# Kernel tuning notes

Measured on AMD Instinct MI355X. Metric: run time of the kernel, lower is better.

Reference implementation:

```python
import jax, jax.numpy as jnp
import numpy as np

B, N, C = 16, 1025, 768          # N = 32*32 patches + 1 CLS token
NUM_HEADS = 12
HEAD_DIM = C // NUM_HEADS        # 64
RED = 2                          # reduction_ratio
NEWTON_ITERS = 6


def setup_inputs() -> dict:
    key = jax.random.key(0)
    ks = jax.random.split(key, 5)
    return {
        "x": jax.random.normal(ks[0], (B, N, C), dtype=jnp.float32),
        "qkv_w": jax.random.normal(ks[1], (3 * C, C), dtype=jnp.float32) * 0.02,
        "qkv_b": jax.random.normal(ks[2], (3 * C,), dtype=jnp.float32) * 0.02,
        "proj_w": jax.random.normal(ks[3], (C, C), dtype=jnp.float32) * 0.02,
        "proj_b": jax.random.normal(ks[4], (C,), dtype=jnp.float32) * 0.02,
    }


def _kernel_gauss(x, y, tau):
    # exp(-||x-y||^2 / tau) via dot-product expansion; x:(B,H,N,D), y:(B,H,M,D)
    x_norm = jnp.sum(x * x, axis=-1, keepdims=True)          # (B,H,N,1)
    y_norm = jnp.sum(y * y, axis=-1, keepdims=True)          # (B,H,M,1)
    dot = jnp.einsum('bhnd,bhmd->bhnm', x, y)
    dist_sq = x_norm + jnp.swapaxes(y_norm, -2, -1) - 2.0 * dot
    return jnp.exp(-dist_sq / tau)


def _newton_inverse(mat, iters):
    # X_{k+1} = X_k (2I - A X_k); init X_0 = A^T / (||A||_inf^2 + eps)
    M = mat.shape[-1]
    I = jnp.eye(M, dtype=mat.dtype)
    norm = jnp.max(jnp.sum(jnp.abs(mat), axis=-1), axis=-1, keepdims=True)[..., None]  # (B,H,1,1)
    inv = jnp.swapaxes(mat, -2, -1) / (norm * norm + 1e-6)
    for _ in range(iters):
        inv = inv @ (2.0 * I - mat @ inv)
    return inv


def _spatial_pool(x, r):
    # avg-pool landmarks: (B,H,S*S,D) -> (B,H,(S//r)^2,D)
    b, h, n, d = x.shape
    s = int(round(n ** 0.5))
    sr = s // r
    x = x.reshape(b, h, sr, r, sr, r, d).mean(axis=(3, 5))
    return x.reshape(b, h, sr * sr, d)


def reference(x, qkv_w, qkv_b, proj_w, proj_b):
    b, n, c = x.shape
    tau = HEAD_DIM ** 0.5
    qkv = (x @ qkv_w.T + qkv_b).reshape(b, n, 3, NUM_HEADS, HEAD_DIM)
    qkv = jnp.transpose(qkv, (2, 0, 3, 1, 4))                # (3,B,H,N,D)
    q, k, v = qkv[0], qkv[1], qkv[2]
    q_cls, q_patch = q[:, :, :1], q[:, :, 1:]
    k_patch = k[:, :, 1:]
    v_patch = v[:, :, 1:]
    q_land = _spatial_pool(q_patch, RED)                     # (B,H,M,D)
    k_land = _spatial_pool(k_patch, RED)
    M1 = _kernel_gauss(q_patch, k_land, tau)                 # (B,H,N-1,M)
    M2 = _kernel_gauss(q_land, k_land, tau)                  # (B,H,M,M)
    M3 = _kernel_gauss(q_land, k_patch, tau)                 # (B,H,M,N-1)
    M2_inv = _newton_inverse(M2, NEWTON_ITERS)
    V_mixed = M2_inv @ (M3 @ v_patch)                        # (B,H,M,D)
    y_patch = M1 @ V_mixed                                   # (B,H,N-1,D)
    y_cls = _kernel_gauss(q_cls, k_land, tau) @ V_mixed      # (B,H,1,D)
    y = jnp.concatenate([y_cls, y_patch], axis=2)            # (B,H,N,D)
    y = jnp.swapaxes(y, 1, 2).reshape(b, n, c)
    return y @ proj_w.T + proj_b
```

## Files before the change

### kernel.cpp

```cpp
#include <hip/hip_runtime.h>

typedef unsigned short u16;

#define NBATCH 16
#define NHEADS 12
#define BH 192
#define NSEQ 1025
#define NP 1024
#define HD 64
#define LM 256
#define INV_TAU 0.125f
#define MROWS 16400
#define MT_X 1032
#define KB768 24
#define XS_ELE ((size_t)MT_X*KB768*64*8)

__device__ __forceinline__ float bf2f(u16 u){
  union { unsigned int i; float f; } x; x.i = ((unsigned int)u)<<16; return x.f;
}
__device__ __forceinline__ u16 f2bf(float f){
  union { float f; unsigned int i; } x; x.f = f;
  unsigned int r = x.i + 0x7fffu + ((x.i >> 16) & 1u);
  return (u16)(r >> 16);
}
__device__ __forceinline__ float ldf(const float* p){ return *p; }
__device__ __forceinline__ float ldf(const u16* p){ return bf2f(*p); }
__device__ __forceinline__ float4 ld4(const float* p){ return *(const float4*)p; }
__device__ __forceinline__ float4 ld4(const u16* p){
  uint2 u = *(const uint2*)p;
  return make_float4(bf2f((u16)u.x), bf2f((u16)(u.x>>16)),
                     bf2f((u16)u.y), bf2f((u16)(u.y>>16)));
}
__device__ __forceinline__ void stf(float* p, float v){ *p = v; }
__device__ __forceinline__ void stf(u16* p, float v){ *p = f2bf(v); }

typedef __attribute__((ext_vector_type(8))) short s8v;
typedef __attribute__((ext_vector_type(4))) float f4v;


__global__ __launch_bounds__(256) void probe_dtype(const u16* __restrict__ x, int* flag)
{
  __shared__ int cnt;
  if (threadIdx.x == 0) cnt = 0;
  __syncthreads();
  int c = 0;
  #pragma unroll
  for (int j = 0; j < 8; ++j){
    u16 u = x[2*(threadIdx.x*8 + j)];
    int e = (u >> 7) & 0xFF;
    if (e >= 100 && e <= 140) c++;
  }
  atomicAdd(&cnt, c);
  __syncthreads();
  if (threadIdx.x == 0) *flag = (cnt > 1024) ? 1 : 0;
}

template<typename TIN>
__global__ __launch_bounds__(256) void cvt_bias(
    const int* __restrict__ flag, int want,
    const TIN* __restrict__ bq_in, const TIN* __restrict__ bp_in,
    float* __restrict__ bq, float* __restrict__ bp)
{
  if (*flag != want) return;
  int i = blockIdx.x*256 + threadIdx.x;
  if (i < 2304) bq[i] = ldf(bq_in + i);
  if (i < 768)  bp[i] = ldf(bp_in + i);
}

template<typename TIN>
__global__ __launch_bounds__(256) void pack_ab(
    const int* __restrict__ flag, int want,
    const TIN* __restrict__ X, int rows_max, int tiles,
    u16* __restrict__ Dh, u16* __restrict__ Dl)
{
  if (*flag != want) return;
  int tid = blockIdx.x*256 + threadIdx.x;
  if (tid >= tiles*KB768*64) return;
  int lane = tid & 63;
  int kb = (tid >> 6) % KB768;
  int mt = tid / (KB768*64);
  int m = mt*16 + (lane & 15); if (m > rows_max-1) m = rows_max-1;
  int k = kb*32 + ((lane>>4) << 3);
  const TIN* src = X + (size_t)m*768 + k;
  float4 a = ld4(src), b = ld4(src + 4);
  float v[8] = {a.x,a.y,a.z,a.w,b.x,b.y,b.z,b.w};
  ushort4 h0,h1,l0,l1;
  u16 h;
  h=f2bf(v[0]); h0.x=h; l0.x=f2bf(v[0]-bf2f(h));
  h=f2bf(v[1]); h0.y=h; l0.y=f2bf(v[1]-bf2f(h));
  h=f2bf(v[2]); h0.z=h; l0.z=f2bf(v[2]-bf2f(h));
  h=f2bf(v[3]); h0.w=h; l0.w=f2bf(v[3]-bf2f(h));
  h=f2bf(v[4]); h1.x=h; l1.x=f2bf(v[4]-bf2f(h));
  h=f2bf(v[5]); h1.y=h; l1.y=f2bf(v[5]-bf2f(h));
  h=f2bf(v[6]); h1.z=h; l1.z=f2bf(v[6]-bf2f(h));
  h=f2bf(v[7]); h1.w=h; l1.w=f2bf(v[7]-bf2f(h));
  size_t o = (size_t)tid*8;
  *(ushort4*)(Dh+o)   = h0; *(ushort4*)(Dh+o+4) = h1;
  *(ushort4*)(Dl+o)   = l0; *(ushort4*)(Dl+o+4) = l1;
}

__global__ __launch_bounds__(256) void qkv_mfma(
    const u16* __restrict__ Xh, const u16* __restrict__ Xl,
    const u16* __restrict__ Wh, const u16* __restrict__ Wl,
    const float* __restrict__ bq,
    float* __restrict__ q, u16* __restrict__ kp, u16* __restrict__ vp)
{
  __shared__ u16 sAh[8*512], sAl[8*512], sBh[4*512], sBl[4*512];
  const int t = threadIdx.x, lane = t & 63, w = t >> 6;
  const int mt0 = blockIdx.x * 8;
  const int by  = blockIdx.y;
  const int nt0 = by * 4;
  const int wr = w >> 1, wc = w & 1;
  f4v acc[4][2];
  #pragma unroll
  for (int a=0;a<4;a++){ acc[a][0]=(f4v){0,0,0,0}; acc[a][1]=(f4v){0,0,0,0}; }
  for (int kb = 0; kb < KB768; ++kb){
    #pragma unroll
    for (int e = 0; e < 6; ++e){
      int cid = e*4 + w;
      const u16* src; u16* dst;
      if (cid < 16){
        int tile = cid >> 1;
        src = ((cid & 1) ? Xl : Xh) + ((size_t)(mt0 + tile)*KB768 + kb)*512 + lane*8;
        dst = ((cid & 1) ? sAl : sAh) + tile*512 + lane*8;
      } else {
        int bc = cid - 16; int tile = bc >> 1;
        src = ((bc & 1) ? Wl : Wh) + ((size_t)(nt0 + tile)*KB768 + kb)*512 + lane*8;
        dst = ((bc & 1) ? sBl : sBh) + tile*512 + lane*8;
      }
      *(uint4*)dst = *(const uint4*)src;
    }
    __syncthreads();
    s8v ah[4], al[4], bh2[2], bl2[2];
    #pragma unroll
    for (int i=0;i<4;i++){
      ah[i] = *(const s8v*)&sAh[(wr*4+i)*512 + lane*8];
      al[i] = *(const s8v*)&sAl[(wr*4+i)*512 + lane*8];
    }
    #pragma unroll
    for (int i=0;i<2;i++){
      bh2[i] = *(const s8v*)&sBh[(wc*2+i)*512 + lane*8];
      bl2[i] = *(const s8v*)&sBl[(wc*2+i)*512 + lane*8];
    }
    #pragma unroll
    for (int mi=0;mi<4;mi++)
      #pragma unroll
      for (int ni=0;ni<2;ni++){
        acc[mi][ni] = __builtin_amdgcn_mfma_f32_16x16x32_bf16(ah[mi], bh2[ni], acc[mi][ni],0,0,0);
        acc[mi][ni] = __builtin_amdgcn_mfma_f32_16x16x32_bf16(al[mi], bh2[ni], acc[mi][ni],0,0,0);
        acc[mi][ni] = __builtin_amdgcn_mfma_f32_16x16x32_bf16(ah[mi], bl2[ni], acc[mi][ni],0,0,0);
      }
    __syncthreads();
  }
  const int which = by / 12, h = by % 12;
  #pragma unroll
  for (int mi=0;mi<4;mi++)
    #pragma unroll
    for (int ni=0;ni<2;ni++){
      int d = (wc*2+ni)*16 + (lane & 15);
      float bias = bq[by*64 + d];
      int mbase = (mt0 + wr*4+mi)*16 + ((lane>>4)<<2);
      #pragma unroll
      for (int r=0;r<4;r++){
        int m = mbase + r;
        if (m >= MROWS) continue;
        float v = acc[mi][ni][r] + bias;
        int b = m / 1025, n = m - b*1025;
        if (which == 0) q[((size_t)(b*12+h)*1025 + n)*64 + d] = v;
        else if (n >= 1){
          size_t idx = ((size_t)(b*12+h)*1024 + (n-1))*64 + d;
          if (which == 1) kp[idx] = f2bf(v); else vp[idx] = f2bf(v);
        }
      }
    }
}

template<typename TOUT>
__global__ __launch_bounds__(256) void proj_mfma(
    const int* __restrict__ flag, int want,
    const u16* __restrict__ Yh, const u16* __restrict__ Yl,
    const u16* __restrict__ Wh, const u16* __restrict__ Wl,
    const float* __restrict__ bp, TOUT* __restrict__ Out)
{
  if (*flag != want) return;
  __shared__ u16 sAh[8*512], sAl[8*512], sBh[4*512], sBl[4*512];
  const int t = threadIdx.x, lane = t & 63, w = t >> 6;
  const int mt0 = blockIdx.x * 8;
  const int by  = blockIdx.y;
  const int nt0 = by * 4;
  const int wr = w >> 1, wc = w & 1;
  f4v acc[4][2];
  #pragma unroll
  for (int a=0;a<4;a++){ acc[a][0]=(f4v){0,0,0,0}; acc[a][1]=(f4v){0,0,0,0}; }
  for (int kb = 0; kb < KB768; ++kb){
    #pragma unroll
    for (int e = 0; e < 6; ++e){
      int cid = e*4 + w;
      const u16* src; u16* dst;
      if (cid < 16){
        int tile = cid >> 1;
        src = ((cid & 1) ? Yl : Yh) + ((size_t)(mt0 + tile)*KB768 + kb)*512 + lane*8;
        dst = ((cid & 1) ? sAl : sAh) + tile*512 + lane*8;
      } else {
        int bc = cid - 16; int tile = bc >> 1;
        src = ((bc & 1) ? Wl : Wh) + ((size_t)(nt0 + tile)*KB768 + kb)*512 + lane*8;
        dst = ((bc & 1) ? sBl : sBh) + tile*512 + lane*8;
      }
      *(uint4*)dst = *(const uint4*)src;
    }
    __syncthreads();
    s8v ah[4], al[4], bh2[2], bl2[2];
    #pragma unroll
    for (int i=0;i<4;i++){
      ah[i] = *(const s8v*)&sAh[(wr*4+i)*512 + lane*8];
      al[i] = *(const s8v*)&sAl[(wr*4+i)*512 + lane*8];
    }
    #pragma unroll
    for (int i=0;i<2;i++){
      bh2[i] = *(const s8v*)&sBh[(wc*2+i)*512 + lane*8];
      bl2[i] = *(const s8v*)&sBl[(wc*2+i)*512 + lane*8];
    }
    #pragma unroll
    for (int mi=0;mi<4;mi++)
      #pragma unroll
      for (int ni=0;ni<2;ni++){
        acc[mi][ni] = __builtin_amdgcn_mfma_f32_16x16x32_bf16(ah[mi], bh2[ni], acc[mi][ni],0,0,0);
        acc[mi][ni] = __builtin_amdgcn_mfma_f32_16x16x32_bf16(al[mi], bh2[ni], acc[mi][ni],0,0,0);
        acc[mi][ni] = __builtin_amdgcn_mfma_f32_16x16x32_bf16(ah[mi], bl2[ni], acc[mi][ni],0,0,0);
      }
    __syncthreads();
  }
  #pragma unroll
  for (int mi=0;mi<4;mi++)
    #pragma unroll
    for (int ni=0;ni<2;ni++){
      int d = (wc*2+ni)*16 + (lane & 15);
      int O = by*64 + d;
      float bias = bp[O];
      int mbase = (mt0 + wr*4+mi)*16 + ((lane>>4)<<2);
      #pragma unroll
      for (int r=0;r<4;r++){
        int m = mbase + r;
        if (m >= MROWS) continue;
        stf(Out + (size_t)m*768 + O, acc[mi][ni][r] + bias);
      }
    }
}

__global__ __launch_bounds__(256) void pack_newtA(
    const float* __restrict__ S, u16* __restrict__ Dh, u16* __restrict__ Dl)
{
  int tid = blockIdx.x*256 + threadIdx.x;
  int lane = tid & 63;
  int kb = (tid>>6) & 7;
  int mt = (tid>>9) & 15;
  int hd = tid >> 13;
  int m = mt*16 + (lane&15);
  int k = kb*32 + ((lane>>4)<<3);
  const float* src = S + (size_t)hd*65536 + m*256 + k;
  float4 a = *(const float4*)src, b = *(const float4*)(src+4);
  float v[8] = {a.x,a.y,a.z,a.w,b.x,b.y,b.z,b.w};
  ushort4 h0,h1,l0,l1; u16 h;
  h=f2bf(v[0]); h0.x=h; l0.x=f2bf(v[0]-bf2f(h));
  h=f2bf(v[1]); h0.y=h; l0.y=f2bf(v[1]-bf2f(h));
  h=f2bf(v[2]); h0.z=h; l0.z=f2bf(v[2]-bf2f(h));
  h=f2bf(v[3]); h0.w=h; l0.w=f2bf(v[3]-bf2f(h));
  h=f2bf(v[4]); h1.x=h; l1.x=f2bf(v[4]-bf2f(h));
  h=f2bf(v[5]); h1.y=h; l1.y=f2bf(v[5]-bf2f(h));
  h=f2bf(v[6]); h1.z=h; l1.z=f2bf(v[6]-bf2f(h));
  h=f2bf(v[7]); h1.w=h; l1.w=f2bf(v[7]-bf2f(h));
  size_t o = (size_t)hd*65536 + (size_t)((mt*8+kb)*64+lane)*8;
  *(ushort4*)(Dh+o)   = h0; *(ushort4*)(Dh+o+4) = h1;
  *(ushort4*)(Dl+o)   = l0; *(ushort4*)(Dl+o+4) = l1;
}

__global__ __launch_bounds__(256) void newton_initP(
    const float* __restrict__ M2g, const float* __restrict__ nrmg,
    u16* __restrict__ Ah, u16* __restrict__ Al,
    u16* __restrict__ Bh, u16* __restrict__ Bl)
{
  __shared__ float T[64][65];
  int hd = blockIdx.x, i0 = blockIdx.y*64, j0 = blockIdx.z*64;
  float nn = nrmg[hd];
  float sc = 1.0f/(nn*nn + 1e-6f);
  const float* Mb = M2g + (size_t)hd*65536;
  size_t hs = (size_t)hd*65536;
  int t = threadIdx.x;
  #pragma unroll
  for (int e=0;e<16;e++){ int f=e*256+t; int r=f>>6, c=f&63; T[r][c] = Mb[(i0+r)*256 + j0+c]; }
  __syncthreads();
  #pragma unroll
  for (int e=0;e<16;e++){
    int f=e*256+t; int r=f>>6, c=f&63;
    float v = T[c][r]*sc;
    int row = j0+r, col = i0+c;
    u16 hv = f2bf(v), lv = f2bf(v - bf2f(hv));
    size_t iA = hs + (size_t)(((row>>4)*8 + (col>>5))*64 + ((row&15)|(((col>>3)&3)<<4)))*8 + (col&7);
    Ah[iA]=hv; Al[iA]=lv;
    size_t iB = hs + (size_t)(((col>>4)*8 + (row>>5))*64 + ((col&15)|(((row>>3)&3)<<4)))*8 + (row&7);
    Bh[iB]=hv; Bl[iB]=lv;
  }
}

template<int MODE>
__global__ __launch_bounds__(256) void mgemmP(
    const u16* __restrict__ Ah_, const u16* __restrict__ Al_,
    const u16* __restrict__ Bh_, const u16* __restrict__ Bl_,
    u16* __restrict__ oAh, u16* __restrict__ oAl,
    u16* __restrict__ oBh, u16* __restrict__ oBl, float* __restrict__ oF)
{
  __shared__ u16 sAh[2048], sAl[2048], sBh[2048], sBl[2048];
  const int t = threadIdx.x, lane = t & 63, w = t >> 6;
  const int hd = blockIdx.x;
  const int mt0 = blockIdx.y * 4, nt0 = blockIdx.z * 4;
  const size_t hs = (size_t)hd * 65536;
  const int wr = w >> 1, wc = w & 1;
  f4v acc[2][2];
  acc[0][0]=(f4v){0,0,0,0}; acc[0][1]=(f4v){0,0,0,0};
  acc[1][0]=(f4v){0,0,0,0}; acc[1][1]=(f4v){0,0,0,0};
  for (int kb = 0; kb < 8; ++kb){
    #pragma unroll
    for (int e = 0; e < 4; ++e){
      int cid = e*4 + w;
      const u16* src; u16* dst;
      if (cid < 8){
        int tile = cid >> 1;
        src = ((cid & 1) ? Al_ : Ah_) + hs + (size_t)((mt0+tile)*8 + kb)*512 + lane*8;
        dst = ((cid & 1) ? sAl : sAh) + tile*512 + lane*8;
      } else {
        int bc = cid - 8; int tile = bc >> 1;
        src = ((bc & 1) ? Bl_ : Bh_) + hs + (size_t)((nt0+tile)*8 + kb)*512 + lane*8;
        dst = ((bc & 1) ? sBl : sBh) + tile*512 + lane*8;
      }
      *(uint4*)dst = *(const uint4*)src;
    }
    __syncthreads();
    s8v a_h[2], a_l[2], b_h[2], b_l[2];
    #pragma unroll
    for (int i=0;i<2;i++){
      a_h[i] = *(const s8v*)&sAh[(wr*2+i)*512 + lane*8];
      a_l[i] = *(const s8v*)&sAl[(wr*2+i)*512 + lane*8];
      b_h[i] = *(const s8v*)&sBh[(wc*2+i)*512 + lane*8];
      b_l[i] = *(const s8v*)&sBl[(wc*2+i)*512 + lane*8];
    }
    #pragma unroll
    for (int mi=0;mi<2;mi++)
      #pragma unroll
      for (int ni=0;ni<2;ni++){
        acc[mi][ni] = __builtin_amdgcn_mfma_f32_16x16x32_bf16(a_h[mi], b_h[ni], acc[mi][ni],0,0,0);
        acc[mi][ni] = __builtin_amdgcn_mfma_f32_16x16x32_bf16(a_l[mi], b_h[ni], acc[mi][ni],0,0,0);
        acc[mi][ni] = __builtin_amdgcn_mfma_f32_16x16x32_bf16(a_h[mi], b_l[ni], acc[mi][ni],0,0,0);
      }
    __syncthreads();
  }
  #pragma unroll
  for (int mi=0;mi<2;mi++)
    #pragma unroll
    for (int ni=0;ni<2;ni++){
      int col = (nt0 + wc*2+ni)*16 + (lane & 15);
      int rowb = (mt0 + wr*2+mi)*16 + ((lane>>4)<<2);
      #pragma unroll
      for (int r=0;r<4;r++){
        int row = rowb + r;
        float v = acc[mi][ni][r];
        if (MODE == 1) v = ((row==col)?2.0f:0.0f) - v;
        if (MODE == 2){
          oF[hs + (size_t)row*256 + col] = v;
        } else {
          u16 hv = f2bf(v), lv = f2bf(v - bf2f(hv));
          if (MODE == 0){
            size_t iA = hs + (size_t)(((row>>4)*8 + (col>>5))*64 + ((row&15)|(((col>>3)&3)<<4)))*8 + (col&7);
            oAh[iA]=hv; oAl[iA]=lv;
          }
          size_t iB = hs + (size_t)(((col>>4)*8 + (row>>5))*64 + ((col&15)|(((row>>3)&3)<<4)))*8 + (row&7);
          oBh[iB]=hv; oBl[iB]=lv;
        }
      }
    }
}

template<typename TIN>
__global__ __launch_bounds__(256) void xpool(
    const int* __restrict__ flag, int want,
    const TIN* __restrict__ X, float* __restrict__ XP)
{
  if (*flag != want) return;
  int idx = blockIdx.x*256 + threadIdx.x;
  if (idx >= NBATCH*LM*768) return;
  int c = idx % 768;
  int l = (idx / 768) & 255;
  int b = idx / (768*256);
  int lr = l >> 4, lc = l & 15;
  int p = lr*64 + lc*2;
  const TIN* xb = X + (size_t)b*NSEQ*768;
  XP[idx] = 0.25f*(ldf(xb + (size_t)(p+1)*768 + c) + ldf(xb + (size_t)(p+2)*768 + c)
                 + ldf(xb + (size_t)(p+33)*768 + c) + ldf(xb + (size_t)(p+34)*768 + c));
}

template<typename TIN>
__global__ __launch_bounds__(256) void lgemm(
    const int* __restrict__ flag, int want,
    const float* __restrict__ XP, const TIN* __restrict__ W, const TIN* __restrict__ Bias,
    int ob, float* __restrict__ OutL)
{
  if (*flag != want) return;
  __shared__ float As[16][68];
  __shared__ float Bs[16][68];
  const int t = threadIdx.x;
  const int m0 = blockIdx.x*64, o0 = blockIdx.y*64;
  const int tm = t>>4, tn = t&15;
  const int la_m = t>>2, la_k = (t&3)<<2;
  float acc[4][4] = {};
  const float* ap0 = XP + (size_t)(m0+la_m)*768 + la_k;
  const TIN* bp0 = W + (size_t)(ob+o0+la_m)*768 + la_k;
  for (int k0 = 0; k0 < 768; k0 += 16){
    float4 a4 = *(const float4*)(ap0 + k0);
    float4 b4 = ld4(bp0 + k0);
    As[la_k+0][la_m]=a4.x; As[la_k+1][la_m]=a4.y; As[la_k+2][la_m]=a4.z; As[la_k+3][la_m]=a4.w;
    Bs[la_k+0][la_m]=b4.x; Bs[la_k+1][la_m]=b4.y; Bs[la_k+2][la_m]=b4.z; Bs[la_k+3][la_m]=b4.w;
    __syncthreads();
    #pragma unroll
    for (int kk = 0; kk < 16; ++kk){
      float4 av = *(const float4*)&As[kk][tm<<2];
      float4 bv = *(const float4*)&Bs[kk][tn<<2];
      float ar[4]={av.x,av.y,av.z,av.w}, br[4]={bv.x,bv.y,bv.z,bv.w};
      #pragma unroll
      for (int ii=0;ii<4;ii++)
        #pragma unroll
        for (int jj=0;jj<4;jj++)
          acc[ii][jj] = fmaf(ar[ii], br[jj], acc[ii][jj]);
    }
    __syncthreads();
  }
  const int h = o0 >> 6;
  #pragma unroll
  for (int ii=0;ii<4;ii++){
    int m = m0 + (tm<<2) + ii;
    int b = m >> 8, l = m & 255;
    #pragma unroll
    for (int jj=0;jj<4;jj++){
      int d = (tn<<2) + jj;
      OutL[((size_t)(b*12+h)*256 + l)*64 + d] = acc[ii][jj] + ldf(Bias + ob + o0 + d);
    }
  }
}

template<typename TIN>
__global__ __launch_bounds__(256) void kvgemm(
    const int* __restrict__ flag, int want,
    const TIN* __restrict__ X, const TIN* __restrict__ W, const TIN* __restrict__ Bias,
    u16* __restrict__ kp, u16* __restrict__ vp)
{
  if (*flag != want) return;
  __shared__ float As[16][68];
  __shared__ float Bs[16][68];
  const int t = threadIdx.x;
  const int m0 = blockIdx.x*64, o0 = blockIdx.y*64;
  const int tm = t>>4, tn = t&15;
  const int la_m = t>>2, la_k = (t&3)<<2;
  float acc[4][4] = {};
  int ar = m0 + la_m;
  int arb = ar >> 10, arn = ar & 1023;
  const TIN* ap0 = X + (size_t)(arb*1025 + arn + 1)*768 + la_k;
  const TIN* bp0 = W + (size_t)(768 + o0 + la_m)*768 + la_k;
  for (int k0 = 0; k0 < 768; k0 += 16){
    float4 a4 = ld4(ap0 + k0);
    float4 b4 = ld4(bp0 + k0);
    As[la_k+0][la_m]=a4.x; As[la_k+1][la_m]=a4.y; As[la_k+2][la_m]=a4.z; As[la_k+3][la_m]=a4.w;
    Bs[la_k+0][la_m]=b4.x; Bs[la_k+1][la_m]=b4.y; Bs[la_k+2][la_m]=b4.z; Bs[la_k+3][la_m]=b4.w;
    __syncthreads();
    #pragma unroll
    for (int kk = 0; kk < 16; ++kk){
      float4 av = *(const float4*)&As[kk][tm<<2];
      float4 bv = *(const float4*)&Bs[kk][tn<<2];
      float arr[4]={av.x,av.y,av.z,av.w}, brr[4]={bv.x,bv.y,bv.z,bv.w};
      #pragma unroll
      for (int ii=0;ii<4;ii++)
        #pragma unroll
        for (int jj=0;jj<4;jj++)
          acc[ii][jj] = fmaf(arr[ii], brr[jj], acc[ii][jj]);
    }
    __syncthreads();
  }
  const int isv = (o0 >= 768);
  const int h = ((o0 - (isv ? 768 : 0)) >> 6);
  u16* dst = isv ? vp : kp;
  #pragma unroll
  for (int ii=0;ii<4;ii++){
    int m = m0 + (tm<<2) + ii;
    int b = m >> 10, n1 = m & 1023;
    #pragma unroll
    for (int jj=0;jj<4;jj++){
      int d = (tn<<2) + jj;
      dst[((size_t)(b*12+h)*1024 + n1)*64 + d] = f2bf(acc[ii][jj] + ldf(Bias + 768 + o0 + d));
    }
  }
}

template<typename TIN>
__global__ __launch_bounds__(256) void qgemm(
    const int* __restrict__ flag, int want,
    const TIN* __restrict__ X, const TIN* __restrict__ W, const TIN* __restrict__ Bias,
    float* __restrict__ q)
{
  if (*flag != want) return;
  __shared__ float As[16][68];
  __shared__ float Bs[16][68];
  const int t = threadIdx.x;
  const int m0 = blockIdx.x*64, o0 = blockIdx.y*64;
  const int tm = t>>4, tn = t&15;
  const int la_m = t>>2, la_k = (t&3)<<2;
  float acc[4][4] = {};
  int am = m0 + la_m; if (am > MROWS-1) am = MROWS-1;
  const TIN* ap0 = X + (size_t)am*768 + la_k;
  const TIN* bp0 = W + (size_t)(o0+la_m)*768 + la_k;
  for (int k0 = 0; k0 < 768; k0 += 16){
    float4 a4 = ld4(ap0 + k0);
    float4 b4 = ld4(bp0 + k0);
    As[la_k+0][la_m]=a4.x; As[la_k+1][la_m]=a4.y; As[la_k+2][la_m]=a4.z; As[la_k+3][la_m]=a4.w;
    Bs[la_k+0][la_m]=b4.x; Bs[la_k+1][la_m]=b4.y; Bs[la_k+2][la_m]=b4.z; Bs[la_k+3][la_m]=b4.w;
    __syncthreads();
    #pragma unroll
    for (int kk = 0; kk < 16; ++kk){
      float4 av = *(const float4*)&As[kk][tm<<2];
      float4 bv = *(const float4*)&Bs[kk][tn<<2];
      float arr[4]={av.x,av.y,av.z,av.w}, brr[4]={bv.x,bv.y,bv.z,bv.w};
      #pragma unroll
      for (int ii=0;ii<4;ii++)
        #pragma unroll
        for (int jj=0;jj<4;jj++)
          acc[ii][jj] = fmaf(arr[ii], brr[jj], acc[ii][jj]);
    }
    __syncthreads();
  }
  const int h = o0 >> 6;
  #pragma unroll
  for (int ii=0;ii<4;ii++){
    int m = m0 + (tm<<2) + ii;
    if (m >= MROWS) break;
    int b = m / 1025, n = m - b*1025;
    #pragma unroll
    for (int jj=0;jj<4;jj++){
      int d = (tn<<2) + jj;
      q[((size_t)(b*12+h)*1025 + n)*64 + d] = acc[ii][jj] + ldf(Bias + o0 + d);
    }
  }
}

template<typename TIN>
__global__ __launch_bounds__(256) void projgemm(
    const int* __restrict__ flag, int want,
    const float* __restrict__ Y, const TIN* __restrict__ W, const TIN* __restrict__ Bias,
    TIN* __restrict__ Out)
{
  if (*flag != want) return;
  __shared__ float As[16][68];
  __shared__ float Bs[16][68];
  const int t = threadIdx.x;
  const int m0 = blockIdx.x*64, o0 = blockIdx.y*64;
  const int tm = t>>4, tn = t&15;
  const int la_m = t>>2, la_k = (t&3)<<2;
  float acc[4][4] = {};
  int am = m0 + la_m; if (am > MROWS-1) am = MROWS-1;
  const float* ap0 = Y + (size_t)am*768 + la_k;
  const TIN* bp0 = W + (size_t)(o0+la_m)*768 + la_k;
  for (int k0 = 0; k0 < 768; k0 += 16){
    float4 a4 = *(const float4*)(ap0 + k0);
    float4 b4 = ld4(bp0 + k0);
    As[la_k+0][la_m]=a4.x; As[la_k+1][la_m]=a4.y; As[la_k+2][la_m]=a4.z; As[la_k+3][la_m]=a4.w;
    Bs[la_k+0][la_m]=b4.x; Bs[la_k+1][la_m]=b4.y; Bs[la_k+2][la_m]=b4.z; Bs[la_k+3][la_m]=b4.w;
    __syncthreads();
    #pragma unroll
    for (int kk = 0; kk < 16; ++kk){
      float4 av = *(const float4*)&As[kk][tm<<2];
      float4 bv = *(const float4*)&Bs[kk][tn<<2];
      float arr[4]={av.x,av.y,av.z,av.w}, brr[4]={bv.x,bv.y,bv.z,bv.w};
      #pragma unroll
      for (int ii=0;ii<4;ii++)
        #pragma unroll
        for (int jj=0;jj<4;jj++)
          acc[ii][jj] = fmaf(arr[ii], brr[jj], acc[ii][jj]);
    }
    __syncthreads();
  }
  #pragma unroll
  for (int ii=0;ii<4;ii++){
    int m = m0 + (tm<<2) + ii;
    if (m >= MROWS) break;
    #pragma unroll
    for (int jj=0;jj<4;jj++){
      int o = o0 + (tn<<2) + jj;
      stf(Out + (size_t)m*768 + o, acc[ii][jj] + ldf(Bias + o));
    }
  }
}

template<int MODE>
__global__ __launch_bounds__(256) void mgemm(
    const float* __restrict__ A, const float* __restrict__ B, float* __restrict__ C)
{
  __shared__ u16 Ah[4*64*8], Al[4*64*8];
  __shared__ u16 Bh[4*64*8], Bl[4*64*8];
  const int t = threadIdx.x;
  const int bh = blockIdx.x;
  const int i0 = blockIdx.y*64, j0 = blockIdx.z*64;
  const float* Ab = A + (size_t)bh*65536;
  const float* Bb = B + (size_t)bh*65536;
  float* Cb = C + (size_t)bh*65536;
  const int lane = t & 63, wave = t >> 6;
  const int wr = wave >> 1, wc = wave & 1;
  f4v acc[2][2];
  acc[0][0]=(f4v){0,0,0,0}; acc[0][1]=(f4v){0,0,0,0};
  acc[1][0]=(f4v){0,0,0,0}; acc[1][1]=(f4v){0,0,0,0};
  for (int k0 = 0; k0 < 256; k0 += 32){
    #pragma unroll
    for (int e = 0; e < 2; ++e){
      int f = e*256 + t;
      int r = f >> 3, c4 = (f & 7) << 2;
      float4 ga = *(const float4*)(Ab + (size_t)(i0+r)*256 + k0 + c4);
      int tile = r >> 4, m = r & 15, quad = c4 >> 3, jq = c4 & 7;
      int dst = ((tile*64 + quad*16 + m)*8 + jq);
      float va[4] = {ga.x, ga.y, ga.z, ga.w};
      ushort4 h4, l4; u16 h;
      h = f2bf(va[0]); h4.x = h; l4.x = f2bf(va[0]-bf2f(h));
      h = f2bf(va[1]); h4.y = h; l4.y = f2bf(va[1]-bf2f(h));
      h = f2bf(va[2]); h4.z = h; l4.z = f2bf(va[2]-bf2f(h));
      h = f2bf(va[3]); h4.w = h; l4.w = f2bf(va[3]-bf2f(h));
      *(ushort4*)&Ah[dst] = h4;
      *(ushort4*)&Al[dst] = l4;
    }
    #pragma unroll
    for (int e = 0; e < 2; ++e){
      int f = e*256 + t;
      int k = f >> 4, c4 = (f & 15) << 2;
      float4 gb = *(const float4*)(Bb + (size_t)(k0+k)*256 + j0 + c4);
      int quad = k >> 3, j = k & 7;
      float vb[4] = {gb.x, gb.y, gb.z, gb.w};
      #pragma unroll
      for (int s = 0; s < 4; ++s){
        int n = c4 + s;
        int idx = (((n>>4)*64 + quad*16 + (n&15))*8 + j);
        u16 h = f2bf(vb[s]);
        Bh[idx] = h;
        Bl[idx] = f2bf(vb[s] - bf2f(h));
      }
    }
    __syncthreads();
    s8v ah[2], al[2], bhf[2], blf[2];
    #pragma unroll
    for (int rt = 0; rt < 2; ++rt){
      int gt = wr*2 + rt;
      ah[rt] = *(const s8v*)&Ah[(gt*64 + lane)*8];
      al[rt] = *(const s8v*)&Al[(gt*64 + lane)*8];
    }
    #pragma unroll
    for (int ct = 0; ct < 2; ++ct){
      int gt = wc*2 + ct;
      bhf[ct] = *(const s8v*)&Bh[(gt*64 + lane)*8];
      blf[ct] = *(const s8v*)&Bl[(gt*64 + lane)*8];
    }
    #pragma unroll
    for (int rt = 0; rt < 2; ++rt)
      #pragma unroll
      for (int ct = 0; ct < 2; ++ct){
        acc[rt][ct] = __builtin_amdgcn_mfma_f32_16x16x32_bf16(ah[rt], bhf[ct], acc[rt][ct], 0,0,0);
        acc[rt][ct] = __builtin_amdgcn_mfma_f32_16x16x32_bf16(al[rt], bhf[ct], acc[rt][ct], 0,0,0);
        acc[rt][ct] = __builtin_amdgcn_mfma_f32_16x16x32_bf16(ah[rt], blf[ct], acc[rt][ct], 0,0,0);
      }
    __syncthreads();
  }
  #pragma unroll
  for (int rt = 0; rt < 2; ++rt)
    #pragma unroll
    for (int ct = 0; ct < 2; ++ct){
      int col = j0 + (wc*2+ct)*16 + (lane & 15);
      int rbase = i0 + (wr*2+rt)*16 + (lane >> 4)*4;
      #pragma unroll
      for (int r = 0; r < 4; ++r){
        int row = rbase + r;
        float v = acc[rt][ct][r];
        if (MODE == 1) v = ((row==col) ? 2.0f : 0.0f) - v;
        Cb[(size_t)row*256 + col] = v;
      }
    }
}

template<int MODE, int NDIM>
__global__ __launch_bounds__(256) void bgemm(
    const float* __restrict__ A, const float* __restrict__ B, float* __restrict__ C)
{
  __shared__ float As[16][68];
  __shared__ float Bs[16][68];
  const int t = threadIdx.x;
  const int bh = blockIdx.x;
  const int i0 = blockIdx.y*64, j0 = blockIdx.z*64;
  const int tm = t>>4, tn = t&15;
  const float* Ab = A + (size_t)bh*65536;
  const float* Bb = B + (size_t)bh*256*NDIM;
  float* Cb = C + (size_t)bh*256*NDIM;
  const int la_m = t>>2, la_k = (t&3)<<2;
  const int lb_k = t>>4, lb_n = (t&15)<<2;
  float acc[4][4] = {};
  for (int k0 = 0; k0 < 256; k0 += 16){
    float4 a4 = *(const float4*)(Ab + (i0+la_m)*256 + k0 + la_k);
    As[la_k+0][la_m]=a4.x; As[la_k+1][la_m]=a4.y; As[la_k+2][la_m]=a4.z; As[la_k+3][la_m]=a4.w;
    *(float4*)&Bs[lb_k][lb_n] = *(const float4*)(Bb + (k0+lb_k)*NDIM + j0 + lb_n);
    __syncthreads();
    #pragma unroll
    for (int kk = 0; kk < 16; ++kk){
      float4 av = *(const float4*)&As[kk][tm<<2];
      float4 bv = *(const float4*)&Bs[kk][tn<<2];
      float arr[4]={av.x,av.y,av.z,av.w}, brr[4]={bv.x,bv.y,bv.z,bv.w};
      #pragma unroll
      for (int ii=0;ii<4;ii++)
        #pragma unroll
        for (int jj=0;jj<4;jj++)
          acc[ii][jj] = fmaf(arr[ii], brr[jj], acc[ii][jj]);
    }
    __syncthreads();
  }
  #pragma unroll
  for (int ii=0;ii<4;ii++){
    int i = i0 + (tm<<2) + ii;
    #pragma unroll
    for (int jj=0;jj<4;jj++){
      int j = j0 + (tn<<2) + jj;
      float v = acc[ii][jj];
      if (MODE == 1) v = ((i==j) ? 2.0f : 0.0f) - v;
      Cb[i*NDIM + j] = v;
    }
  }
}

__global__ __launch_bounds__(256) void gauss_m2(
    const float* __restrict__ Q, const float* __restrict__ K,
    const float* __restrict__ qn, const float* __restrict__ kn, float* __restrict__ Out)
{
  __shared__ float Qs[64][68];
  __shared__ float Kst[64][66];
  const int bh = blockIdx.x, i0 = blockIdx.y*64, j0 = blockIdx.z*64;
  const int t = threadIdx.x, tm = t>>4, tn = t&15;
  #pragma unroll
  for (int e=0;e<4;e++){
    int f = e*256 + t; int r = f>>4; int c4 = (f&15)<<2;
    *(float4*)&Qs[r][c4] = *(const float4*)(Q + (size_t)(bh*256 + i0 + r)*64 + c4);
    float4 k4 = *(const float4*)(K + (size_t)(bh*256 + j0 + r)*64 + c4);
    Kst[c4+0][r]=k4.x; Kst[c4+1][r]=k4.y; Kst[c4+2][r]=k4.z; Kst[c4+3][r]=k4.w;
  }
  __syncthreads();
  float d[4][4] = {};
  for (int k0=0;k0<64;k0+=4){
    float qv[4][4], kv[4][4];
    #pragma unroll
    for (int ii=0;ii<4;ii++){
      float4 q4 = *(const float4*)&Qs[(tm<<2)+ii][k0];
      qv[ii][0]=q4.x; qv[ii][1]=q4.y; qv[ii][2]=q4.z; qv[ii][3]=q4.w;
    }
    #pragma unroll
    for (int kk=0;kk<4;kk++)
      #pragma unroll
      for (int jj=0;jj<4;jj++)
        kv[kk][jj] = Kst[k0+kk][(tn<<2)+jj];
    #pragma unroll
    for (int ii=0;ii<4;ii++)
      #pragma unroll
      for (int jj=0;jj<4;jj++){
        d[ii][jj] = fmaf(qv[ii][0], kv[0][jj], d[ii][jj]);
        d[ii][jj] = fmaf(qv[ii][1], kv[1][jj], d[ii][jj]);
        d[ii][jj] = fmaf(qv[ii][2], kv[2][jj], d[ii][jj]);
        d[ii][jj] = fmaf(qv[ii][3], kv[3][jj], d[ii][jj]);
      }
  }
  float qnr[4], knc[4];
  #pragma unroll
  for (int ii=0;ii<4;ii++) qnr[ii] = qn[bh*256 + i0 + (tm<<2) + ii];
  #pragma unroll
  for (int jj=0;jj<4;jj++) knc[jj] = kn[bh*256 + j0 + (tn<<2) + jj];
  #pragma unroll
  for (int ii=0;ii<4;ii++)
    #pragma unroll
    for (int jj=0;jj<4;jj++)
      Out[(size_t)(bh*256 + i0 + (tm<<2) + ii)*256 + j0 + (tn<<2) + jj] =
        __expf(-(qnr[ii] + knc[jj] - 2.0f*d[ii][jj]) * INV_TAU);
}

template<int YMODE, int RQ, int RK, typename TQ, typename TK, typename TV>
__global__ __launch_bounds__(256) void gauss_av(
    const TQ* __restrict__ Q, const TK* __restrict__ Km,
    const TV* __restrict__ V, const float* __restrict__ qn,
    const float* __restrict__ kn, float* __restrict__ Out)
{
  __shared__ float Qs[64][68];
  __shared__ float Kst[64][66];
  __shared__ float Ss[64][68];
  const int bh = blockIdx.x, i0 = blockIdx.y*64;
  const int t = threadIdx.x, tm = t>>4, tn = t&15;
  #pragma unroll
  for (int e=0;e<4;e++){
    int f = e*256 + t; int r = f>>4; int c4 = (f&15)<<2;
    int gi = i0 + r; if (gi > RQ-1) gi = RQ-1;
    *(float4*)&Qs[r][c4] = ld4(Q + (size_t)(bh*RQ + gi)*64 + c4);
  }
  float qnr[4];
  #pragma unroll
  for (int ii=0;ii<4;ii++){ int gi = i0 + (tm<<2) + ii; if (gi > RQ-1) gi = RQ-1; qnr[ii] = qn[bh*RQ + gi]; }
  float acc[4][4] = {};
  for (int j0 = 0; j0 < RK; j0 += 64){
    __syncthreads();
    #pragma unroll
    for (int e=0;e<4;e++){
      int f = e*256 + t; int r = f>>4; int c4 = (f&15)<<2;
      float4 k4 = ld4(Km + (size_t)(bh*RK + j0 + r)*64 + c4);
      Kst[c4+0][r]=k4.x; Kst[c4+1][r]=k4.y; Kst[c4+2][r]=k4.z; Kst[c4+3][r]=k4.w;
    }
    __syncthreads();
    float d[4][4] = {};
    for (int k0=0;k0<64;k0+=4){
      float qv[4][4], kv[4][4];
      #pragma unroll
      for (int ii=0;ii<4;ii++){
        float4 q4 = *(const float4*)&Qs[(tm<<2)+ii][k0];
        qv[ii][0]=q4.x; qv[ii][1]=q4.y; qv[ii][2]=q4.z; qv[ii][3]=q4.w;
      }
      #pragma unroll
      for (int kk=0;kk<4;kk++)
        #pragma unroll
        for (int jj=0;jj<4;jj++)
          kv[kk][jj] = Kst[k0+kk][(tn<<2)+jj];
      #pragma unroll
      for (int ii=0;ii<4;ii++)
        #pragma unroll
        for (int jj=0;jj<4;jj++){
          d[ii][jj] = fmaf(qv[ii][0], kv[0][jj], d[ii][jj]);
          d[ii][jj] = fmaf(qv[ii][1], kv[1][jj], d[ii][jj]);
          d[ii][jj] = fmaf(qv[ii][2], kv[2][jj], d[ii][jj]);
          d[ii][jj] = fmaf(qv[ii][3], kv[3][jj], d[ii][jj]);
        }
    }
    float knc[4];
    #pragma unroll
    for (int jj=0;jj<4;jj++) knc[jj] = kn[bh*RK + j0 + (tn<<2) + jj];
    #pragma unroll
    for (int ii=0;ii<4;ii++)
      #pragma unroll
      for (int jj=0;jj<4;jj++)
        Ss[(tm<<2)+ii][(tn<<2)+jj] = __expf(-(qnr[ii] + knc[jj] - 2.0f*d[ii][jj]) * INV_TAU);
    __syncthreads();
    const TV* Vb = V + (size_t)(bh*RK + j0)*64;
    for (int c0=0;c0<64;c0+=4){
      float sv[4][4], vv[4][4];
      #pragma unroll
      for (int ii=0;ii<4;ii++){
        float4 s4 = *(const float4*)&Ss[(tm<<2)+ii][c0];
        sv[ii][0]=s4.x; sv[ii][1]=s4.y; sv[ii][2]=s4.z; sv[ii][3]=s4.w;
      }
      #pragma unroll
      for (int cc=0;cc<4;cc++){
        float4 v4 = ld4(Vb + (c0+cc)*64 + (tn<<2));
        vv[cc][0]=v4.x; vv[cc][1]=v4.y; vv[cc][2]=v4.z; vv[cc][3]=v4.w;
      }
      #pragma unroll
      for (int ii=0;ii<4;ii++)
        #pragma unroll
        for (int jj=0;jj<4;jj++){
          acc[ii][jj] = fmaf(sv[ii][0], vv[0][jj], acc[ii][jj]);
          acc[ii][jj] = fmaf(sv[ii][1], vv[1][jj], acc[ii][jj]);
          acc[ii][jj] = fmaf(sv[ii][2], vv[2][jj], acc[ii][jj]);
          acc[ii][jj] = fmaf(sv[ii][3], vv[3][jj], acc[ii][jj]);
        }
    }
  }
  #pragma unroll
  for (int ii=0;ii<4;ii++){
    int i = i0 + (tm<<2) + ii;
    if (i < RQ){
      if (YMODE == 1){
        int b = bh / 12, h = bh - b*12;
        float* ob = Out + (size_t)(b*1025 + i)*768 + h*64 + (tn<<2);
        ob[0]=acc[ii][0]; ob[1]=acc[ii][1]; ob[2]=acc[ii][2]; ob[3]=acc[ii][3];
      } else if (YMODE == 2){
        int b = bh / 12, h = bh - b*12;
        int ym = b*1025 + i;
        int c = h*64 + (tn<<2);
        int mt = ym >> 4, mrem = ym & 15;
        int kb = c >> 5, q8 = (c >> 3) & 3, j = c & 7;
        int lanep = mrem + (q8 << 4);
        size_t o = ((size_t)(mt*KB768 + kb)*64 + lanep)*8 + j;
        u16* Yh = (u16*)Out;
        u16* Yl = Yh + XS_ELE;
        ushort4 hv, lv; u16 h2;
        h2=f2bf(acc[ii][0]); hv.x=h2; lv.x=f2bf(acc[ii][0]-bf2f(h2));
        h2=f2bf(acc[ii][1]); hv.y=h2; lv.y=f2bf(acc[ii][1]-bf2f(h2));
        h2=f2bf(acc[ii][2]); hv.z=h2; lv.z=f2bf(acc[ii][2]-bf2f(h2));
        h2=f2bf(acc[ii][3]); hv.w=h2; lv.w=f2bf(acc[ii][3]-bf2f(h2));
        *(ushort4*)(Yh + o) = hv;
        *(ushort4*)(Yl + o) = lv;
      } else {
        float* ob = Out + (size_t)(bh*RQ + i)*64 + (tn<<2);
        ob[0]=acc[ii][0]; ob[1]=acc[ii][1]; ob[2]=acc[ii][2]; ob[3]=acc[ii][3];
      }
    }
  }
}

template<typename T>
__global__ __launch_bounds__(256) void rownorm(
    const T* __restrict__ x, float* __restrict__ out, int rows)
{
  int gt = blockIdx.x*256 + threadIdx.x;
  int w = gt >> 6, lane = gt & 63;
  if (w >= rows) return;
  float v = ldf(x + (size_t)w*64 + lane);
  float s = v*v;
  #pragma unroll
  for (int off=32; off>0; off>>=1) s += __shfl_xor(s, off, 64);
  if (lane == 0) out[w] = s;
}

__global__ __launch_bounds__(256) void m2norm(
    const float* __restrict__ M2, float* __restrict__ nrm)
{
  __shared__ float red[256];
  int bh = blockIdx.x, i = threadIdx.x;
  const float* r = M2 + ((size_t)bh*256 + i)*256;
  float s = 0.f;
  for (int j=0;j<256;j++) s += fabsf(r[j]);
  red[i] = s; __syncthreads();
  for (int st=128; st>0; st>>=1){
    if (i < st) red[i] = fmaxf(red[i], red[i+st]);
    __syncthreads();
  }
  if (i == 0) nrm[bh] = red[0];
}

__global__ __launch_bounds__(256) void newton_init(
    const float* __restrict__ M2, const float* __restrict__ nrm, float* __restrict__ inv)
{
  __shared__ float T[64][65];
  int bh = blockIdx.x, i0 = blockIdx.y*64, j0 = blockIdx.z*64;
  float nn = nrm[bh];
  float sc = 1.0f/(nn*nn + 1e-6f);
  const float* Mb = M2 + (size_t)bh*65536;
  float* ob = inv + (size_t)bh*65536;
  int t = threadIdx.x;
  #pragma unroll
  for (int e=0;e<16;e++){ int f=e*256+t; int r=f>>6, c=f&63; T[r][c] = Mb[(i0+r)*256 + j0+c]; }
  __syncthreads();
  #pragma unroll
  for (int e=0;e<16;e++){ int f=e*256+t; int r=f>>6, c=f&63; ob[(j0+r)*256 + i0+c] = T[c][r]*sc; }
}

__global__ __launch_bounds__(256) void diag_fill(u16* out, int n, float val)
{
  int i = blockIdx.x*256 + threadIdx.x;
  if (i < n) out[i] = f2bf(val);
}

extern "C" void kernel_launch(void* const* d_in, const int* in_sizes, int n_in,
                              void* d_out, int out_size, void* d_ws, size_t ws_size,
                              hipStream_t stream)
{
  const float* xf = (const float*)d_in[0]; const u16* xb = (const u16*)d_in[0];
  const float* wf = (const float*)d_in[1]; const u16* wb = (const u16*)d_in[1];
  const float* bf = (const float*)d_in[2]; const u16* bb = (const u16*)d_in[2];
  const float* pwf= (const float*)d_in[3]; const u16* pwb= (const u16*)d_in[3];
  const float* pbf= (const float*)d_in[4]; const u16* pbb= (const u16*)d_in[4];
  #define DUAL(kf, kb2) do { kf; kb2; } while(0)

  int* flag = (int*)d_ws;
  probe_dtype<<<1, 256, 0, stream>>>((const u16*)d_in[0], flag);

  {
    char* base = (char*)d_ws;
    size_t off = 256;
    auto A = [&](size_t bytes)->char*{ char* r = base + off; off += (bytes + 255) & ~(size_t)255; return r; };
    u16*  Xh = (u16*)A(XS_ELE*2);
    u16*  Xl = (u16*)A(XS_ELE*2);
    float* q  = (float*)A((size_t)BH*NSEQ*64*4);
    char*  KT = A((size_t)6*32*65536*2*2);
    float* XP = (float*)A((size_t)NBATCH*LM*768*4);
    float* QL = (float*)A((size_t)BH*LM*64*4);
    float* KL = (float*)A((size_t)BH*LM*64*4);
    u16*  Wqh = (u16*)A((size_t)144*KB768*64*8*2);
    u16*  Wql = (u16*)A((size_t)144*KB768*64*8*2);
    u16*  Wph = (u16*)A((size_t)48*KB768*64*8*2);
    u16*  Wpl = (u16*)A((size_t)48*KB768*64*8*2);
    float* curF = (float*)A((size_t)32*65536*4);
    float* bq  = (float*)A(2304*4);
    float* bp  = (float*)A(768*4);
    float* qn  = (float*)A((size_t)BH*NSEQ*4);
    float* qln = (float*)A((size_t)BH*LM*4);
    float* kln = (float*)A((size_t)BH*LM*4);
    float* kpn = (float*)A((size_t)BH*NP*4);
    float* nrm = (float*)A(256*4);
    if (ws_size >= off){
      float* M2 = (float*)Xh;
      u16*  Yh = Xh;
      u16*  Yl = Xh + XS_ELE;
      float* KV = XP;
      float* Vm = QL;
      u16* kp = (u16*)KT;
      u16* vp = (u16*)(KT + (size_t)BH*NP*64*2);
      const size_t PB = (size_t)32*65536;
      u16* nb = (u16*)KT;
      u16 *curAh = nb + 0*2*PB, *curAl = curAh + PB;
      u16 *curBh = nb + 1*2*PB, *curBl = curBh + PB;
      u16 *TsBh  = nb + 2*2*PB, *TsBl  = TsBh  + PB;
      u16 *nxtAh = nb + 3*2*PB, *nxtAl = nxtAh + PB;
      u16 *nxtBh = nb + 4*2*PB, *nxtBl = nxtBh + PB;
      u16 *M2Ah  = nb + 5*2*PB, *M2Al  = M2Ah  + PB;

      DUAL((cvt_bias<float><<<9,256,0,stream>>>(flag,0,bf,pbf,bq,bp)),
           (cvt_bias<u16>  <<<9,256,0,stream>>>(flag,1,bb,pbb,bq,bp)));
      DUAL((pack_ab<float><<<MT_X*KB768*64/256,256,0,stream>>>(flag,0,xf,MROWS,MT_X,Xh,Xl)),
           (pack_ab<u16>  <<<MT_X*KB768*64/256,256,0,stream>>>(flag,1,xb,MROWS,MT_X,Xh,Xl)));
      DUAL((pack_ab<float><<<144*KB768*64/256,256,0,stream>>>(flag,0,wf,2304,144,Wqh,Wql)),
           (pack_ab<u16>  <<<144*KB768*64/256,256,0,stream>>>(flag,1,wb,2304,144,Wqh,Wql)));
      DUAL((pack_ab<float><<<48*KB768*64/256,256,0,stream>>>(flag,0,pwf,768,48,Wph,Wpl)),
           (pack_ab<u16>  <<<48*KB768*64/256,256,0,stream>>>(flag,1,pwb,768,48,Wph,Wpl)));
      qkv_mfma<<<dim3(129,36),256,0,stream>>>(Xh,Xl,Wqh,Wql,bq,q,kp,vp);
      DUAL((xpool<float><<<(NBATCH*LM*768)/256,256,0,stream>>>(flag,0,xf,XP)),
           (xpool<u16>  <<<(NBATCH*LM*768)/256,256,0,stream>>>(flag,1,xb,XP)));
      DUAL((lgemm<float><<<dim3(64,12),256,0,stream>>>(flag,0,XP,wf,bf,0,QL)),
           (lgemm<u16>  <<<dim3(64,12),256,0,stream>>>(flag,1,XP,wb,bb,0,QL)));
      DUAL((lgemm<float><<<dim3(64,12),256,0,stream>>>(flag,0,XP,wf,bf,768,KL)),
           (lgemm<u16>  <<<dim3(64,12),256,0,stream>>>(flag,1,XP,wb,bb,768,KL)));
      rownorm<float><<<(BH*LM*64)/256,256,0,stream>>>(QL, qln, BH*LM);
      rownorm<float><<<(BH*LM*64)/256,256,0,stream>>>(KL, kln, BH*LM);
      rownorm<float><<<(BH*NSEQ*64)/256,256,0,stream>>>(q, qn, BH*NSEQ);
      rownorm<u16><<<(BH*NP*64)/256,256,0,stream>>>(kp, kpn, BH*NP);
      gauss_m2<<<dim3(BH,4,4),256,0,stream>>>(QL, KL, qln, kln, M2);
      m2norm<<<BH,256,0,stream>>>(M2, nrm);
      gauss_av<0,256,1024,float,u16,u16><<<dim3(BH,4),256,0,stream>>>(QL, kp, vp, qln, kpn, KV);
      for (int g = 0; g < 6; ++g){
        const float* M2g = M2 + (size_t)g*32*65536;
        pack_newtA<<<1024,256,0,stream>>>(M2g, M2Ah, M2Al);
        newton_initP<<<dim3(32,4,4),256,0,stream>>>(M2g, nrm+g*32, curAh,curAl,curBh,curBl);
        for (int it = 0; it < 6; ++it){
          mgemmP<1><<<dim3(32,4,4),256,0,stream>>>(M2Ah,M2Al,curBh,curBl,
                                                   nullptr,nullptr,TsBh,TsBl,nullptr);
          if (it < 5){
            mgemmP<0><<<dim3(32,4,4),256,0,stream>>>(curAh,curAl,TsBh,TsBl,
                                                     nxtAh,nxtAl,nxtBh,nxtBl,nullptr);
            u16* t0;
            t0=curAh; curAh=nxtAh; nxtAh=t0;  t0=curAl; curAl=nxtAl; nxtAl=t0;
            t0=curBh; curBh=nxtBh; nxtBh=t0;  t0=curBl; curBl=nxtBl; nxtBl=t0;
          } else {
            mgemmP<2><<<dim3(32,4,4),256,0,stream>>>(curAh,curAl,TsBh,TsBl,
                                                     nullptr,nullptr,nullptr,nullptr,curF);
          }
        }
        bgemm<0,64><<<dim3(32,4,1),256,0,stream>>>(curF, KV + (size_t)g*32*16384,
                                                   Vm + (size_t)g*32*16384);
      }
      gauss_av<2,1025,256,float,float,float><<<dim3(BH,17),256,0,stream>>>(
          q, KL, Vm, qn, kln, (float*)Yh);
      DUAL((proj_mfma<float><<<dim3(129,12),256,0,stream>>>(flag,0,Yh,Yl,Wph,Wpl,bp,(float*)d_out)),
           (proj_mfma<u16>  <<<dim3(129,12),256,0,stream>>>(flag,1,Yh,Yl,Wph,Wpl,bp,(u16*)d_out)));
      return;
    }
  }

  {
    char* base = (char*)d_ws;
    size_t off = 256;
    auto A = [&](size_t bytes)->char*{ char* r = base + off; off += (bytes + 255) & ~(size_t)255; return r; };
    float* XP   = (float*)A((size_t)NBATCH*LM*768*4);
    float* QL   = (float*)A((size_t)BH*LM*64*4);
    float* KL   = (float*)A((size_t)BH*LM*64*4);
    char*  M2Y  = A((size_t)MROWS*768*4);
    char*  KPV  = A((size_t)MROWS*768*4);
    float* qn   = (float*)A((size_t)BH*NSEQ*4);
    float* qln  = (float*)A((size_t)BH*LM*4);
    float* kln  = (float*)A((size_t)BH*LM*4);
    float* kpn  = (float*)A((size_t)BH*NP*4);
    float* nrm  = (float*)A(256*4);
    if (ws_size < off){
      diag_fill<<<(out_size+255)/256, 256, 0, stream>>>((u16*)d_out, out_size, (float)(ws_size >> 20));
      return;
    }
    float* M2 = (float*)M2Y;
    float* y  = (float*)M2Y;
    float* KV = XP;
    float* Vm = QL;
    u16*   kp = (u16*)KPV;
    u16*   vp = (u16*)(KPV + (size_t)BH*NP*64*2);
    float* T0 = (float*)KPV;
    float* T1 = T0 + (size_t)64*65536;
    float* T2 = T0 + (size_t)128*65536;
    float* q  = (float*)KPV;

    DUAL((xpool<float><<<(NBATCH*LM*768)/256,256,0,stream>>>(flag,0,xf,XP)),
         (xpool<u16>  <<<(NBATCH*LM*768)/256,256,0,stream>>>(flag,1,xb,XP)));
    DUAL((lgemm<float><<<dim3(64,12),256,0,stream>>>(flag,0,XP,wf,bf,0,QL)),
         (lgemm<u16>  <<<dim3(64,12),256,0,stream>>>(flag,1,XP,wb,bb,0,QL)));
    DUAL((lgemm<float><<<dim3(64,12),256,0,stream>>>(flag,0,XP,wf,bf,768,KL)),
         (lgemm<u16>  <<<dim3(64,12),256,0,stream>>>(flag,1,XP,wb,bb,768,KL)));
    rownorm<float><<<(BH*LM*64)/256,256,0,stream>>>(QL, qln, BH*LM);
    rownorm<float><<<(BH*LM*64)/256,256,0,stream>>>(KL, kln, BH*LM);
    gauss_m2<<<dim3(BH,4,4),256,0,stream>>>(QL, KL, qln, kln, M2);
    m2norm<<<BH,256,0,stream>>>(M2, nrm);
    DUAL((kvgemm<float><<<dim3(256,24),256,0,stream>>>(flag,0,xf,wf,bf,kp,vp)),
         (kvgemm<u16>  <<<dim3(256,24),256,0,stream>>>(flag,1,xb,wb,bb,kp,vp)));
    rownorm<u16><<<(BH*NP*64)/256,256,0,stream>>>(kp, kpn, BH*NP);
    gauss_av<0,256,1024,float,u16,u16><<<dim3(BH,4),256,0,stream>>>(QL, kp, vp, qln, kpn, KV);
    for (int g = 0; g < 3; ++g){
      const float* M2g = M2 + (size_t)g*64*65536;
      newton_init<<<dim3(64,4,4),256,0,stream>>>(M2g, nrm + g*64, T0);
      float* cur = T0; float* nxt = T2;
      for (int it = 0; it < 6; ++it){
        mgemm<1><<<dim3(64,4,4),256,0,stream>>>(M2g, cur, T1);
        mgemm<0><<<dim3(64,4,4),256,0,stream>>>(cur, T1, nxt);
        float* tt = cur; cur = nxt; nxt = tt;
      }
      bgemm<0,64><<<dim3(64,4,1),256,0,stream>>>(cur, KV + (size_t)g*64*16384,
                                                 Vm + (size_t)g*64*16384);
    }
    DUAL((qgemm<float><<<dim3(257,12),256,0,stream>>>(flag,0,xf,wf,bf,q)),
         (qgemm<u16>  <<<dim3(257,12),256,0,stream>>>(flag,1,xb,wb,bb,q)));
    rownorm<float><<<(BH*NSEQ*64)/256,256,0,stream>>>(q, qn, BH*NSEQ);
    gauss_av<1,1025,256,float,float,float><<<dim3(BH,17),256,0,stream>>>(q, KL, Vm, qn, kln, y);
    DUAL((projgemm<float><<<dim3(257,12),256,0,stream>>>(flag,0,y,pwf,pbf,(float*)d_out)),
         (projgemm<u16>  <<<dim3(257,12),256,0,stream>>>(flag,1,y,pwb,pbb,(u16*)d_out)));
  }
}
```

Before: 2.346 ms.

## Move Gaussian attention products to split-bf16 MFMA and drop the scalar fallback path

Replaces the scalar FMA gauss_av kernel with an MFMA version that splits Q into high and low bf16 parts and reads K/V stored in MFMA fragment layouts. The qkv projection epilogue now writes K and V directly in those packed layouts, and new pack kernels prepare the landmark K and mixed-V operands. The old fp32 fallback path (kvgemm, qgemm, projgemm, mgemm) is deleted, and the GEMM grids are transposed so blocks that share a weight tile run next to each other. Precision of the K/V terms falls to a single bf16 part in some products, and the extra pack kernels add launches and memory traffic.

```diff
diff --git a/kernel.cpp b/kernel.cpp
--- a/kernel.cpp
+++ b/kernel.cpp
@@ -107,8 +107,8 @@
 {
   __shared__ u16 sAh[8*512], sAl[8*512], sBh[4*512], sBl[4*512];
   const int t = threadIdx.x, lane = t & 63, w = t >> 6;
-  const int mt0 = blockIdx.x * 8;
-  const int by  = blockIdx.y;
+  const int by  = blockIdx.x;
+  const int mt0 = blockIdx.y * 8;
   const int nt0 = by * 4;
   const int wr = w >> 1, wc = w & 1;
   f4v acc[4][2];
@@ -166,10 +166,19 @@
         if (m >= MROWS) continue;
         float v = acc[mi][ni][r] + bias;
         int b = m / 1025, n = m - b*1025;
-        if (which == 0) q[((size_t)(b*12+h)*1025 + n)*64 + d] = v;
+        int bh = b*12 + h;
+        if (which == 0) q[((size_t)bh*1025 + n)*64 + d] = v;
         else if (n >= 1){
-          size_t idx = ((size_t)(b*12+h)*1024 + (n-1))*64 + d;
-          if (which == 1) kp[idx] = f2bf(v); else vp[idx] = f2bf(v);
+          int kr = n - 1;
+          if (which == 1){
+            size_t idx = (size_t)bh*65536 +
+              (size_t)((((kr>>4)*2 + (d>>5))*64) + ((kr&15)|(((d>>3)&3)<<4)))*8 + (d&7);
+            kp[idx] = f2bf(v);
+          } else {
+            size_t idx = (size_t)bh*65536 +
+              (size_t)((((kr>>5)*4 + (d>>4))*64) + ((d&15)|(((kr>>3)&3)<<4)))*8 + (kr&7);
+            vp[idx] = f2bf(v);
+          }
         }
       }
     }
@@ -185,8 +194,8 @@
   if (*flag != want) return;
   __shared__ u16 sAh[8*512], sAl[8*512], sBh[4*512], sBl[4*512];
   const int t = threadIdx.x, lane = t & 63, w = t >> 6;
-  const int mt0 = blockIdx.x * 8;
-  const int by  = blockIdx.y;
+  const int by  = blockIdx.x;
+  const int mt0 = blockIdx.y * 8;
   const int nt0 = by * 4;
   const int wr = w >> 1, wc = w & 1;
   f4v acc[4][2];
@@ -445,244 +454,56 @@
   }
 }
 
-template<typename TIN>
-__global__ __launch_bounds__(256) void kvgemm(
-    const int* __restrict__ flag, int want,
-    const TIN* __restrict__ X, const TIN* __restrict__ W, const TIN* __restrict__ Bias,
-    u16* __restrict__ kp, u16* __restrict__ vp)
-{
-  if (*flag != want) return;
-  __shared__ float As[16][68];
-  __shared__ float Bs[16][68];
-  const int t = threadIdx.x;
-  const int m0 = blockIdx.x*64, o0 = blockIdx.y*64;
-  const int tm = t>>4, tn = t&15;
-  const int la_m = t>>2, la_k = (t&3)<<2;
-  float acc[4][4] = {};
-  int ar = m0 + la_m;
-  int arb = ar >> 10, arn = ar & 1023;
-  const TIN* ap0 = X + (size_t)(arb*1025 + arn + 1)*768 + la_k;
-  const TIN* bp0 = W + (size_t)(768 + o0 + la_m)*768 + la_k;
-  for (int k0 = 0; k0 < 768; k0 += 16){
-    float4 a4 = ld4(ap0 + k0);
-    float4 b4 = ld4(bp0 + k0);
-    As[la_k+0][la_m]=a4.x; As[la_k+1][la_m]=a4.y; As[la_k+2][la_m]=a4.z; As[la_k+3][la_m]=a4.w;
-    Bs[la_k+0][la_m]=b4.x; Bs[la_k+1][la_m]=b4.y; Bs[la_k+2][la_m]=b4.z; Bs[la_k+3][la_m]=b4.w;
-    __syncthreads();
-    #pragma unroll
-    for (int kk = 0; kk < 16; ++kk){
-      float4 av = *(const float4*)&As[kk][tm<<2];
-      float4 bv = *(const float4*)&Bs[kk][tn<<2];
-      float arr[4]={av.x,av.y,av.z,av.w}, brr[4]={bv.x,bv.y,bv.z,bv.w};
-      #pragma unroll
-      for (int ii=0;ii<4;ii++)
-        #pragma unroll
-        for (int jj=0;jj<4;jj++)
-          acc[ii][jj] = fmaf(arr[ii], brr[jj], acc[ii][jj]);
-    }
-    __syncthreads();
-  }
-  const int isv = (o0 >= 768);
-  const int h = ((o0 - (isv ? 768 : 0)) >> 6);
-  u16* dst = isv ? vp : kp;
-  #pragma unroll
-  for (int ii=0;ii<4;ii++){
-    int m = m0 + (tm<<2) + ii;
-    int b = m >> 10, n1 = m & 1023;
-    #pragma unroll
-    for (int jj=0;jj<4;jj++){
-      int d = (tn<<2) + jj;
-      dst[((size_t)(b*12+h)*1024 + n1)*64 + d] = f2bf(acc[ii][jj] + ldf(Bias + 768 + o0 + d));
-    }
-  }
-}
-
-template<typename TIN>
-__global__ __launch_bounds__(256) void qgemm(
-    const int* __restrict__ flag, int want,
-    const TIN* __restrict__ X, const TIN* __restrict__ W, const TIN* __restrict__ Bias,
-    float* __restrict__ q)
-{
-  if (*flag != want) return;
-  __shared__ float As[16][68];
-  __shared__ float Bs[16][68];
-  const int t = threadIdx.x;
-  const int m0 = blockIdx.x*64, o0 = blockIdx.y*64;
-  const int tm = t>>4, tn = t&15;
-  const int la_m = t>>2, la_k = (t&3)<<2;
-  float acc[4][4] = {};
-  int am = m0 + la_m; if (am > MROWS-1) am = MROWS-1;
-  const TIN* ap0 = X + (size_t)am*768 + la_k;
-  const TIN* bp0 = W + (size_t)(o0+la_m)*768 + la_k;
-  for (int k0 = 0; k0 < 768; k0 += 16){
-    float4 a4 = ld4(ap0 + k0);
-    float4 b4 = ld4(bp0 + k0);
-    As[la_k+0][la_m]=a4.x; As[la_k+1][la_m]=a4.y; As[la_k+2][la_m]=a4.z; As[la_k+3][la_m]=a4.w;
-    Bs[la_k+0][la_m]=b4.x; Bs[la_k+1][la_m]=b4.y; Bs[la_k+2][la_m]=b4.z; Bs[la_k+3][la_m]=b4.w;
-    __syncthreads();
-    #pragma unroll
-    for (int kk = 0; kk < 16; ++kk){
-      float4 av = *(const float4*)&As[kk][tm<<2];
-      float4 bv = *(const float4*)&Bs[kk][tn<<2];
-      float arr[4]={av.x,av.y,av.z,av.w}, brr[4]={bv.x,bv.y,bv.z,bv.w};
-      #pragma unroll
-      for (int ii=0;ii<4;ii++)
-        #pragma unroll
-        for (int jj=0;jj<4;jj++)
-          acc[ii][jj] = fmaf(arr[ii], brr[jj], acc[ii][jj]);
-    }
-    __syncthreads();
-  }
-  const int h = o0 >> 6;
-  #pragma unroll
-  for (int ii=0;ii<4;ii++){
-    int m = m0 + (tm<<2) + ii;
-    if (m >= MROWS) break;
-    int b = m / 1025, n = m - b*1025;
-    #pragma unroll
-    for (int jj=0;jj<4;jj++){
-      int d = (tn<<2) + jj;
-      q[((size_t)(b*12+h)*1025 + n)*64 + d] = acc[ii][jj] + ldf(Bias + o0 + d);
-    }
-  }
-}
-
-template<typename TIN>
-__global__ __launch_bounds__(256) void projgemm(
-    const int* __restrict__ flag, int want,
-    const float* __restrict__ Y, const TIN* __restrict__ W, const TIN* __restrict__ Bias,
-    TIN* __restrict__ Out)
-{
-  if (*flag != want) return;
-  __shared__ float As[16][68];
-  __shared__ float Bs[16][68];
-  const int t = threadIdx.x;
-  const int m0 = blockIdx.x*64, o0 = blockIdx.y*64;
-  const int tm = t>>4, tn = t&15;
-  const int la_m = t>>2, la_k = (t&3)<<2;
-  float acc[4][4] = {};
-  int am = m0 + la_m; if (am > MROWS-1) am = MROWS-1;
-  const float* ap0 = Y + (size_t)am*768 + la_k;
-  const TIN* bp0 = W + (size_t)(o0+la_m)*768 + la_k;
-  for (int k0 = 0; k0 < 768; k0 += 16){
-    float4 a4 = *(const float4*)(ap0 + k0);
-    float4 b4 = ld4(bp0 + k0);
-    As[la_k+0][la_m]=a4.x; As[la_k+1][la_m]=a4.y; As[la_k+2][la_m]=a4.z; As[la_k+3][la_m]=a4.w;
-    Bs[la_k+0][la_m]=b4.x; Bs[la_k+1][la_m]=b4.y; Bs[la_k+2][la_m]=b4.z; Bs[la_k+3][la_m]=b4.w;
-    __syncthreads();
-    #pragma unroll
-    for (int kk = 0; kk < 16; ++kk){
-      float4 av = *(const float4*)&As[kk][tm<<2];
-      float4 bv = *(const float4*)&Bs[kk][tn<<2];
-      float arr[4]={av.x,av.y,av.z,av.w}, brr[4]={bv.x,bv.y,bv.z,bv.w};
-      #pragma unroll
-      for (int ii=0;ii<4;ii++)
-        #pragma unroll
-        for (int jj=0;jj<4;jj++)
-          acc[ii][jj] = fmaf(arr[ii], brr[jj], acc[ii][jj]);
-    }
-    __syncthreads();
-  }
-  #pragma unroll
-  for (int ii=0;ii<4;ii++){
-    int m = m0 + (tm<<2) + ii;
-    if (m >= MROWS) break;
-    #pragma unroll
-    for (int jj=0;jj<4;jj++){
-      int o = o0 + (tn<<2) + jj;
-      stf(Out + (size_t)m*768 + o, acc[ii][jj] + ldf(Bias + o));
-    }
-  }
-}
-
-template<int MODE>
-__global__ __launch_bounds__(256) void mgemm(
-    const float* __restrict__ A, const float* __restrict__ B, float* __restrict__ C)
-{
-  __shared__ u16 Ah[4*64*8], Al[4*64*8];
-  __shared__ u16 Bh[4*64*8], Bl[4*64*8];
-  const int t = threadIdx.x;
-  const int bh = blockIdx.x;
-  const int i0 = blockIdx.y*64, j0 = blockIdx.z*64;
-  const float* Ab = A + (size_t)bh*65536;
-  const float* Bb = B + (size_t)bh*65536;
-  float* Cb = C + (size_t)bh*65536;
-  const int lane = t & 63, wave = t >> 6;
-  const int wr = wave >> 1, wc = wave & 1;
-  f4v acc[2][2];
-  acc[0][0]=(f4v){0,0,0,0}; acc[0][1]=(f4v){0,0,0,0};
-  acc[1][0]=(f4v){0,0,0,0}; acc[1][1]=(f4v){0,0,0,0};
-  for (int k0 = 0; k0 < 256; k0 += 32){
-    #pragma unroll
-    for (int e = 0; e < 2; ++e){
-      int f = e*256 + t;
-      int r = f >> 3, c4 = (f & 7) << 2;
-      float4 ga = *(const float4*)(Ab + (size_t)(i0+r)*256 + k0 + c4);
-      int tile = r >> 4, m = r & 15, quad = c4 >> 3, jq = c4 & 7;
-      int dst = ((tile*64 + quad*16 + m)*8 + jq);
-      float va[4] = {ga.x, ga.y, ga.z, ga.w};
-      ushort4 h4, l4; u16 h;
-      h = f2bf(va[0]); h4.x = h; l4.x = f2bf(va[0]-bf2f(h));
-      h = f2bf(va[1]); h4.y = h; l4.y = f2bf(va[1]-bf2f(h));
-      h = f2bf(va[2]); h4.z = h; l4.z = f2bf(va[2]-bf2f(h));
-      h = f2bf(va[3]); h4.w = h; l4.w = f2bf(va[3]-bf2f(h));
-      *(ushort4*)&Ah[dst] = h4;
-      *(ushort4*)&Al[dst] = l4;
-    }
-    #pragma unroll
-    for (int e = 0; e < 2; ++e){
-      int f = e*256 + t;
-      int k = f >> 4, c4 = (f & 15) << 2;
-      float4 gb = *(const float4*)(Bb + (size_t)(k0+k)*256 + j0 + c4);
-      int quad = k >> 3, j = k & 7;
-      float vb[4] = {gb.x, gb.y, gb.z, gb.w};
-      #pragma unroll
-      for (int s = 0; s < 4; ++s){
-        int n = c4 + s;
-        int idx = (((n>>4)*64 + quad*16 + (n&15))*8 + j);
-        u16 h = f2bf(vb[s]);
-        Bh[idx] = h;
-        Bl[idx] = f2bf(vb[s] - bf2f(h));
-      }
-    }
-    __syncthreads();
-    s8v ah[2], al[2], bhf[2], blf[2];
-    #pragma unroll
-    for (int rt = 0; rt < 2; ++rt){
-      int gt = wr*2 + rt;
-      ah[rt] = *(const s8v*)&Ah[(gt*64 + lane)*8];
-      al[rt] = *(const s8v*)&Al[(gt*64 + lane)*8];
-    }
-    #pragma unroll
-    for (int ct = 0; ct < 2; ++ct){
-      int gt = wc*2 + ct;
-      bhf[ct] = *(const s8v*)&Bh[(gt*64 + lane)*8];
-      blf[ct] = *(const s8v*)&Bl[(gt*64 + lane)*8];
-    }
-    #pragma unroll
-    for (int rt = 0; rt < 2; ++rt)
-      #pragma unroll
-      for (int ct = 0; ct < 2; ++ct){
-        acc[rt][ct] = __builtin_amdgcn_mfma_f32_16x16x32_bf16(ah[rt], bhf[ct], acc[rt][ct], 0,0,0);
-        acc[rt][ct] = __builtin_amdgcn_mfma_f32_16x16x32_bf16(al[rt], bhf[ct], acc[rt][ct], 0,0,0);
-        acc[rt][ct] = __builtin_amdgcn_mfma_f32_16x16x32_bf16(ah[rt], blf[ct], acc[rt][ct], 0,0,0);
-      }
-    __syncthreads();
-  }
-  #pragma unroll
-  for (int rt = 0; rt < 2; ++rt)
-    #pragma unroll
-    for (int ct = 0; ct < 2; ++ct){
-      int col = j0 + (wc*2+ct)*16 + (lane & 15);
-      int rbase = i0 + (wr*2+rt)*16 + (lane >> 4)*4;
-      #pragma unroll
-      for (int r = 0; r < 4; ++r){
-        int row = rbase + r;
-        float v = acc[rt][ct][r];
-        if (MODE == 1) v = ((row==col) ? 2.0f : 0.0f) - v;
-        Cb[(size_t)row*256 + col] = v;
-      }
-    }
+__global__ __launch_bounds__(256) void gauss_m2(
+    const float* __restrict__ Q, const float* __restrict__ K,
+    const float* __restrict__ qn, const float* __restrict__ kn, float* __restrict__ Out)
+{
+  __shared__ float Qs[64][68];
+  __shared__ float Kst[64][66];
+  const int bh = blockIdx.x, i0 = blockIdx.y*64, j0 = blockIdx.z*64;
+  const int t = threadIdx.x, tm = t>>4, tn = t&15;
+  #pragma unroll
+  for (int e=0;e<4;e++){
+    int f = e*256 + t; int r = f>>4; int c4 = (f&15)<<2;
+    *(float4*)&Qs[r][c4] = *(const float4*)(Q + (size_t)(bh*256 + i0 + r)*64 + c4);
+    float4 k4 = *(const float4*)(K + (size_t)(bh*256 + j0 + r)*64 + c4);
+    Kst[c4+0][r]=k4.x; Kst[c4+1][r]=k4.y; Kst[c4+2][r]=k4.z; Kst[c4+3][r]=k4.w;
+  }
+  __syncthreads();
+  float d[4][4] = {};
+  for (int k0=0;k0<64;k0+=4){
+    float qv[4][4], kv[4][4];
+    #pragma unroll
+    for (int ii=0;ii<4;ii++){
+      float4 q4 = *(const float4*)&Qs[(tm<<2)+ii][k0];
+      qv[ii][0]=q4.x; qv[ii][1]=q4.y; qv[ii][2]=q4.z; qv[ii][3]=q4.w;
+    }
+    #pragma unroll
+    for (int kk=0;kk<4;kk++)
+      #pragma unroll
+      for (int jj=0;jj<4;jj++)
+        kv[kk][jj] = Kst[k0+kk][(tn<<2)+jj];
+    #pragma unroll
+    for (int ii=0;ii<4;ii++)
+      #pragma unroll
+      for (int jj=0;jj<4;jj++){
+        d[ii][jj] = fmaf(qv[ii][0], kv[0][jj], d[ii][jj]);
+        d[ii][jj] = fmaf(qv[ii][1], kv[1][jj], d[ii][jj]);
+        d[ii][jj] = fmaf(qv[ii][2], kv[2][jj], d[ii][jj]);
+        d[ii][jj] = fmaf(qv[ii][3], kv[3][jj], d[ii][jj]);
+      }
+  }
+  float qnr[4], knc[4];
+  #pragma unroll
+  for (int ii=0;ii<4;ii++) qnr[ii] = qn[bh*256 + i0 + (tm<<2) + ii];
+  #pragma unroll
+  for (int jj=0;jj<4;jj++) knc[jj] = kn[bh*256 + j0 + (tn<<2) + jj];
+  #pragma unroll
+  for (int ii=0;ii<4;ii++)
+    #pragma unroll
+    for (int jj=0;jj<4;jj++)
+      Out[(size_t)(bh*256 + i0 + (tm<<2) + ii)*256 + j0 + (tn<<2) + jj] =
+        __expf(-(qnr[ii] + knc[jj] - 2.0f*d[ii][jj]) * INV_TAU);
 }
 
 template<int MODE, int NDIM>
@@ -732,174 +553,193 @@
   }
 }
 
-__global__ __launch_bounds__(256) void gauss_m2(
-    const float* __restrict__ Q, const float* __restrict__ K,
-    const float* __restrict__ qn, const float* __restrict__ kn, float* __restrict__ Out)
-{
-  __shared__ float Qs[64][68];
-  __shared__ float Kst[64][66];
-  const int bh = blockIdx.x, i0 = blockIdx.y*64, j0 = blockIdx.z*64;
-  const int t = threadIdx.x, tm = t>>4, tn = t&15;
-  #pragma unroll
-  for (int e=0;e<4;e++){
-    int f = e*256 + t; int r = f>>4; int c4 = (f&15)<<2;
-    *(float4*)&Qs[r][c4] = *(const float4*)(Q + (size_t)(bh*256 + i0 + r)*64 + c4);
-    float4 k4 = *(const float4*)(K + (size_t)(bh*256 + j0 + r)*64 + c4);
-    Kst[c4+0][r]=k4.x; Kst[c4+1][r]=k4.y; Kst[c4+2][r]=k4.z; Kst[c4+3][r]=k4.w;
-  }
-  __syncthreads();
-  float d[4][4] = {};
-  for (int k0=0;k0<64;k0+=4){
-    float qv[4][4], kv[4][4];
-    #pragma unroll
-    for (int ii=0;ii<4;ii++){
-      float4 q4 = *(const float4*)&Qs[(tm<<2)+ii][k0];
-      qv[ii][0]=q4.x; qv[ii][1]=q4.y; qv[ii][2]=q4.z; qv[ii][3]=q4.w;
-    }
-    #pragma unroll
-    for (int kk=0;kk<4;kk++)
-      #pragma unroll
-      for (int jj=0;jj<4;jj++)
-        kv[kk][jj] = Kst[k0+kk][(tn<<2)+jj];
-    #pragma unroll
-    for (int ii=0;ii<4;ii++)
-      #pragma unroll
-      for (int jj=0;jj<4;jj++){
-        d[ii][jj] = fmaf(qv[ii][0], kv[0][jj], d[ii][jj]);
-        d[ii][jj] = fmaf(qv[ii][1], kv[1][jj], d[ii][jj]);
-        d[ii][jj] = fmaf(qv[ii][2], kv[2][jj], d[ii][jj]);
-        d[ii][jj] = fmaf(qv[ii][3], kv[3][jj], d[ii][jj]);
-      }
-  }
-  float qnr[4], knc[4];
-  #pragma unroll
-  for (int ii=0;ii<4;ii++) qnr[ii] = qn[bh*256 + i0 + (tm<<2) + ii];
-  #pragma unroll
-  for (int jj=0;jj<4;jj++) knc[jj] = kn[bh*256 + j0 + (tn<<2) + jj];
-  #pragma unroll
-  for (int ii=0;ii<4;ii++)
-    #pragma unroll
-    for (int jj=0;jj<4;jj++)
-      Out[(size_t)(bh*256 + i0 + (tm<<2) + ii)*256 + j0 + (tn<<2) + jj] =
-        __expf(-(qnr[ii] + knc[jj] - 2.0f*d[ii][jj]) * INV_TAU);
-}
-
-template<int YMODE, int RQ, int RK, typename TQ, typename TK, typename TV>
-__global__ __launch_bounds__(256) void gauss_av(
-    const TQ* __restrict__ Q, const TK* __restrict__ Km,
-    const TV* __restrict__ V, const float* __restrict__ qn,
-    const float* __restrict__ kn, float* __restrict__ Out)
-{
-  __shared__ float Qs[64][68];
-  __shared__ float Kst[64][66];
-  __shared__ float Ss[64][68];
+template<int YMODE, int RQ, int RK, int KSPLIT, int VSPLIT>
+__global__ __launch_bounds__(256) void gauss_av_m(
+    const float* __restrict__ Q,
+    const u16* __restrict__ Kh, const u16* __restrict__ Kl,
+    const u16* __restrict__ Vh, const u16* __restrict__ Vl,
+    const float* __restrict__ qn, const float* __restrict__ kn,
+    float* __restrict__ Out)
+{
+  __shared__ u16 Ph[4096], Pl[4096];
   const int bh = blockIdx.x, i0 = blockIdx.y*64;
-  const int t = threadIdx.x, tm = t>>4, tn = t&15;
-  #pragma unroll
-  for (int e=0;e<4;e++){
-    int f = e*256 + t; int r = f>>4; int c4 = (f&15)<<2;
-    int gi = i0 + r; if (gi > RQ-1) gi = RQ-1;
-    *(float4*)&Qs[r][c4] = ld4(Q + (size_t)(bh*RQ + gi)*64 + c4);
-  }
-  float qnr[4];
-  #pragma unroll
-  for (int ii=0;ii<4;ii++){ int gi = i0 + (tm<<2) + ii; if (gi > RQ-1) gi = RQ-1; qnr[ii] = qn[bh*RQ + gi]; }
-  float acc[4][4] = {};
+  const int t = threadIdx.x, lane = t&63, w = t>>6, wr = w>>1, wc = w&1;
+  const size_t kbase = (size_t)bh*RK*64;
+  s8v qfh[2][2], qfl[2][2];
+  #pragma unroll
+  for (int mi=0;mi<2;mi++){
+    int row = i0 + (wr*2+mi)*16 + (lane&15);
+    if (row > RQ-1) row = RQ-1;
+    const float* src = Q + ((size_t)bh*RQ + row)*64 + ((lane>>4)<<3);
+    #pragma unroll
+    for (int kb=0;kb<2;kb++){
+      float4 a = *(const float4*)(src + kb*32);
+      float4 b = *(const float4*)(src + kb*32 + 4);
+      float v[8]={a.x,a.y,a.z,a.w,b.x,b.y,b.z,b.w};
+      union { s8v v8; u16 u[8]; } H, L;
+      #pragma unroll
+      for (int j=0;j<8;j++){ u16 hh=f2bf(v[j]); H.u[j]=hh; L.u[j]=f2bf(v[j]-bf2f(hh)); }
+      qfh[mi][kb]=H.v8; qfl[mi][kb]=L.v8;
+    }
+  }
+  float qnr[2][4];
+  #pragma unroll
+  for (int mi=0;mi<2;mi++)
+    #pragma unroll
+    for (int rr=0;rr<4;rr++){
+      int row = i0 + (wr*2+mi)*16 + ((lane>>4)<<2) + rr;
+      if (row > RQ-1) row = RQ-1;
+      qnr[mi][rr] = qn[(size_t)bh*RQ + row];
+    }
+  f4v oacc[2][2];
+  oacc[0][0]=(f4v){0,0,0,0}; oacc[0][1]=(f4v){0,0,0,0};
+  oacc[1][0]=(f4v){0,0,0,0}; oacc[1][1]=(f4v){0,0,0,0};
+
   for (int j0 = 0; j0 < RK; j0 += 64){
-    __syncthreads();
-    #pragma unroll
-    for (int e=0;e<4;e++){
-      int f = e*256 + t; int r = f>>4; int c4 = (f&15)<<2;
-      float4 k4 = ld4(Km + (size_t)(bh*RK + j0 + r)*64 + c4);
-      Kst[c4+0][r]=k4.x; Kst[c4+1][r]=k4.y; Kst[c4+2][r]=k4.z; Kst[c4+3][r]=k4.w;
-    }
-    __syncthreads();
-    float d[4][4] = {};
-    for (int k0=0;k0<64;k0+=4){
-      float qv[4][4], kv[4][4];
-      #pragma unroll
-      for (int ii=0;ii<4;ii++){
-        float4 q4 = *(const float4*)&Qs[(tm<<2)+ii][k0];
-        qv[ii][0]=q4.x; qv[ii][1]=q4.y; qv[ii][2]=q4.z; qv[ii][3]=q4.w;
-      }
-      #pragma unroll
-      for (int kk=0;kk<4;kk++)
+    s8v kfh[2][2], kfl[2][2];
+    #pragma unroll
+    for (int ci=0;ci<2;ci++){
+      int ntg = (j0>>4) + wc*2 + ci;
+      #pragma unroll
+      for (int kb=0;kb<2;kb++){
+        size_t a = kbase + (size_t)((ntg*2+kb)*64 + lane)*8;
+        kfh[ci][kb] = *(const s8v*)(Kh + a);
+        if (KSPLIT) kfl[ci][kb] = *(const s8v*)(Kl + a);
+      }
+    }
+    f4v sacc[2][2];
+    sacc[0][0]=(f4v){0,0,0,0}; sacc[0][1]=(f4v){0,0,0,0};
+    sacc[1][0]=(f4v){0,0,0,0}; sacc[1][1]=(f4v){0,0,0,0};
+    #pragma unroll
+    for (int mi=0;mi<2;mi++)
+      #pragma unroll
+      for (int ci=0;ci<2;ci++)
         #pragma unroll
-        for (int jj=0;jj<4;jj++)
-          kv[kk][jj] = Kst[k0+kk][(tn<<2)+jj];
-      #pragma unroll
-      for (int ii=0;ii<4;ii++)
+        for (int kb=0;kb<2;kb++){
+          sacc[mi][ci] = __builtin_amdgcn_mfma_f32_16x16x32_bf16(qfh[mi][kb], kfh[ci][kb], sacc[mi][ci],0,0,0);
+          sacc[mi][ci] = __builtin_amdgcn_mfma_f32_16x16x32_bf16(qfl[mi][kb], kfh[ci][kb], sacc[mi][ci],0,0,0);
+          if (KSPLIT)
+            sacc[mi][ci] = __builtin_amdgcn_mfma_f32_16x16x32_bf16(qfh[mi][kb], kfl[ci][kb], sacc[mi][ci],0,0,0);
+        }
+    float knc[2];
+    #pragma unroll
+    for (int ci=0;ci<2;ci++)
+      knc[ci] = kn[(size_t)bh*RK + j0 + (wc*2+ci)*16 + (lane&15)];
+    #pragma unroll
+    for (int mi=0;mi<2;mi++)
+      #pragma unroll
+      for (int ci=0;ci<2;ci++){
+        int cl = (wc*2+ci)*16 + (lane&15);
         #pragma unroll
-        for (int jj=0;jj<4;jj++){
-          d[ii][jj] = fmaf(qv[ii][0], kv[0][jj], d[ii][jj]);
-          d[ii][jj] = fmaf(qv[ii][1], kv[1][jj], d[ii][jj]);
-          d[ii][jj] = fmaf(qv[ii][2], kv[2][jj], d[ii][jj]);
-          d[ii][jj] = fmaf(qv[ii][3], kv[3][jj], d[ii][jj]);
+        for (int rr=0;rr<4;rr++){
+          int rl = (wr*2+mi)*16 + ((lane>>4)<<2) + rr;
+          float p = __expf(-(qnr[mi][rr] + knc[ci] - 2.0f*sacc[mi][ci][rr]) * INV_TAU);
+          int ad = (((rl>>4)*2 + (cl>>5))*64 + ((rl&15)|(((cl>>3)&3)<<4)))*8 + (cl&7);
+          u16 hh = f2bf(p);
+          Ph[ad] = hh; Pl[ad] = f2bf(p - bf2f(hh));
         }
-    }
-    float knc[4];
-    #pragma unroll
-    for (int jj=0;jj<4;jj++) knc[jj] = kn[bh*RK + j0 + (tn<<2) + jj];
-    #pragma unroll
-    for (int ii=0;ii<4;ii++)
-      #pragma unroll
-      for (int jj=0;jj<4;jj++)
-        Ss[(tm<<2)+ii][(tn<<2)+jj] = __expf(-(qnr[ii] + knc[jj] - 2.0f*d[ii][jj]) * INV_TAU);
-    __syncthreads();
-    const TV* Vb = V + (size_t)(bh*RK + j0)*64;
-    for (int c0=0;c0<64;c0+=4){
-      float sv[4][4], vv[4][4];
-      #pragma unroll
-      for (int ii=0;ii<4;ii++){
-        float4 s4 = *(const float4*)&Ss[(tm<<2)+ii][c0];
-        sv[ii][0]=s4.x; sv[ii][1]=s4.y; sv[ii][2]=s4.z; sv[ii][3]=s4.w;
-      }
-      #pragma unroll
-      for (int cc=0;cc<4;cc++){
-        float4 v4 = ld4(Vb + (c0+cc)*64 + (tn<<2));
-        vv[cc][0]=v4.x; vv[cc][1]=v4.y; vv[cc][2]=v4.z; vv[cc][3]=v4.w;
-      }
-      #pragma unroll
-      for (int ii=0;ii<4;ii++)
+      }
+    __syncthreads();
+    s8v pfh[2][2], pfl[2][2];
+    #pragma unroll
+    for (int mi=0;mi<2;mi++)
+      #pragma unroll
+      for (int kb=0;kb<2;kb++){
+        int ad = (((wr*2+mi)*2 + kb)*64 + lane)*8;
+        pfh[mi][kb] = *(const s8v*)&Ph[ad];
+        pfl[mi][kb] = *(const s8v*)&Pl[ad];
+      }
+    s8v vfh[2][2], vfl[2][2];
+    #pragma unroll
+    for (int ni=0;ni<2;ni++){
+      int nt = wc*2 + ni;
+      #pragma unroll
+      for (int kb=0;kb<2;kb++){
+        int kbg = (j0>>5) + kb;
+        size_t a = kbase + (size_t)((kbg*4 + nt)*64 + lane)*8;
+        vfh[ni][kb] = *(const s8v*)(Vh + a);
+        if (VSPLIT) vfl[ni][kb] = *(const s8v*)(Vl + a);
+      }
+    }
+    #pragma unroll
+    for (int mi=0;mi<2;mi++)
+      #pragma unroll
+      for (int ni=0;ni<2;ni++)
         #pragma unroll
-        for (int jj=0;jj<4;jj++){
-          acc[ii][jj] = fmaf(sv[ii][0], vv[0][jj], acc[ii][jj]);
-          acc[ii][jj] = fmaf(sv[ii][1], vv[1][jj], acc[ii][jj]);
-          acc[ii][jj] = fmaf(sv[ii][2], vv[2][jj], acc[ii][jj]);
-          acc[ii][jj] = fmaf(sv[ii][3], vv[3][jj], acc[ii][jj]);
+        for (int kb=0;kb<2;kb++){
+          oacc[mi][ni] = __builtin_amdgcn_mfma_f32_16x16x32_bf16(pfh[mi][kb], vfh[ni][kb], oacc[mi][ni],0,0,0);
+          oacc[mi][ni] = __builtin_amdgcn_mfma_f32_16x16x32_bf16(pfl[mi][kb], vfh[ni][kb], oacc[mi][ni],0,0,0);
+          if (VSPLIT)
+            oacc[mi][ni] = __builtin_amdgcn_mfma_f32_16x16x32_bf16(pfh[mi][kb], vfl[ni][kb], oacc[mi][ni],0,0,0);
         }
-    }
-  }
-  #pragma unroll
-  for (int ii=0;ii<4;ii++){
-    int i = i0 + (tm<<2) + ii;
-    if (i < RQ){
-      if (YMODE == 1){
-        int b = bh / 12, h = bh - b*12;
-        float* ob = Out + (size_t)(b*1025 + i)*768 + h*64 + (tn<<2);
-        ob[0]=acc[ii][0]; ob[1]=acc[ii][1]; ob[2]=acc[ii][2]; ob[3]=acc[ii][3];
-      } else if (YMODE == 2){
-        int b = bh / 12, h = bh - b*12;
-        int ym = b*1025 + i;
-        int c = h*64 + (tn<<2);
-        int mt = ym >> 4, mrem = ym & 15;
-        int kb = c >> 5, q8 = (c >> 3) & 3, j = c & 7;
-        int lanep = mrem + (q8 << 4);
-        size_t o = ((size_t)(mt*KB768 + kb)*64 + lanep)*8 + j;
-        u16* Yh = (u16*)Out;
-        u16* Yl = Yh + XS_ELE;
-        ushort4 hv, lv; u16 h2;
-        h2=f2bf(acc[ii][0]); hv.x=h2; lv.x=f2bf(acc[ii][0]-bf2f(h2));
-        h2=f2bf(acc[ii][1]); hv.y=h2; lv.y=f2bf(acc[ii][1]-bf2f(h2));
-        h2=f2bf(acc[ii][2]); hv.z=h2; lv.z=f2bf(acc[ii][2]-bf2f(h2));
-        h2=f2bf(acc[ii][3]); hv.w=h2; lv.w=f2bf(acc[ii][3]-bf2f(h2));
-        *(ushort4*)(Yh + o) = hv;
-        *(ushort4*)(Yl + o) = lv;
-      } else {
-        float* ob = Out + (size_t)(bh*RQ + i)*64 + (tn<<2);
-        ob[0]=acc[ii][0]; ob[1]=acc[ii][1]; ob[2]=acc[ii][2]; ob[3]=acc[ii][3];
-      }
-    }
+    __syncthreads();
+  }
+  #pragma unroll
+  for (int mi=0;mi<2;mi++)
+    #pragma unroll
+    for (int ni=0;ni<2;ni++){
+      int d = (wc*2+ni)*16 + (lane&15);
+      #pragma unroll
+      for (int rr=0;rr<4;rr++){
+        int i = i0 + (wr*2+mi)*16 + ((lane>>4)<<2) + rr;
+        if (i >= RQ) continue;
+        float v = oacc[mi][ni][rr];
+        if (YMODE == 0){
+          Out[((size_t)bh*RQ + i)*64 + d] = v;
+        } else {
+          int b = bh/12, h = bh - b*12;
+          int ym = b*1025 + i;
+          int c = h*64 + d;
+          size_t idx = ((size_t)((ym>>4)*KB768 + (c>>5))*64 + ((ym&15)|(((c>>3)&3)<<4)))*8 + (c&7);
+          u16* Yh = (u16*)Out; u16* Yl = Yh + XS_ELE;
+          u16 hh = f2bf(v);
+          Yh[idx] = hh; Yl[idx] = f2bf(v - bf2f(hh));
+        }
+      }
+    }
+}
+
+__global__ __launch_bounds__(256) void pack_bKL(
+    const float* __restrict__ KL, u16* __restrict__ Dh, u16* __restrict__ Dl)
+{
+  int tid = blockIdx.x*256 + threadIdx.x;
+  int bh = tid >> 11, rem = tid & 2047;
+  int lane = rem & 63, kb = (rem>>6)&1, ntg = rem>>7;
+  int krow = ntg*16 + (lane&15);
+  int d0 = kb*32 + ((lane>>4)<<3);
+  const float* src = KL + ((size_t)bh*256 + krow)*64 + d0;
+  float4 a = *(const float4*)src, b = *(const float4*)(src+4);
+  float v[8] = {a.x,a.y,a.z,a.w,b.x,b.y,b.z,b.w};
+  ushort4 h0,h1,l0,l1; u16 h;
+  h=f2bf(v[0]); h0.x=h; l0.x=f2bf(v[0]-bf2f(h));
+  h=f2bf(v[1]); h0.y=h; l0.y=f2bf(v[1]-bf2f(h));
+  h=f2bf(v[2]); h0.z=h; l0.z=f2bf(v[2]-bf2f(h));
+  h=f2bf(v[3]); h0.w=h; l0.w=f2bf(v[3]-bf2f(h));
+  h=f2bf(v[4]); h1.x=h; l1.x=f2bf(v[4]-bf2f(h));
+  h=f2bf(v[5]); h1.y=h; l1.y=f2bf(v[5]-bf2f(h));
+  h=f2bf(v[6]); h1.z=h; l1.z=f2bf(v[6]-bf2f(h));
+  h=f2bf(v[7]); h1.w=h; l1.w=f2bf(v[7]-bf2f(h));
+  size_t o = (size_t)tid*8;
+  *(ushort4*)(Dh+o)   = h0; *(ushort4*)(Dh+o+4) = h1;
+  *(ushort4*)(Dl+o)   = l0; *(ushort4*)(Dl+o+4) = l1;
+}
+
+__global__ __launch_bounds__(256) void pack_bVm(
+    const float* __restrict__ Vm, u16* __restrict__ Dh, u16* __restrict__ Dl)
+{
+  int tid = blockIdx.x*256 + threadIdx.x;
+  int bh = tid >> 11, rem = tid & 2047;
+  int lane = rem & 63, nt = (rem>>6)&3, kbg = rem>>8;
+  int d = nt*16 + (lane&15);
+  int kr0 = kbg*32 + ((lane>>4)<<3);
+  float v[8];
+  #pragma unroll
+  for (int j=0;j<8;j++) v[j] = Vm[((size_t)bh*256 + kr0 + j)*64 + d];
+  size_t o = (size_t)tid*8;
+  #pragma unroll
+  for (int j=0;j<8;j++){
+    u16 h = f2bf(v[j]);
+    Dh[o+j] = h; Dl[o+j] = f2bf(v[j]-bf2f(h));
   }
 }
 
@@ -915,6 +755,22 @@
   #pragma unroll
   for (int off=32; off>0; off>>=1) s += __shfl_xor(s, off, 64);
   if (lane == 0) out[w] = s;
+}
+
+__global__ __launch_bounds__(256) void rownorm_kpack(
+    const u16* __restrict__ Kp, float* __restrict__ out)
+{
+  int gt = blockIdx.x*256 + threadIdx.x;
+  int wv = gt >> 6, d = gt & 63;
+  if (wv >= BH*NP) return;
+  int bh = wv >> 10, kr = wv & 1023;
+  size_t a = (size_t)bh*65536 +
+    (size_t)((((kr>>4)*2 + (d>>5))*64) + ((kr&15)|(((d>>3)&3)<<4)))*8 + (d&7);
+  float v = bf2f(Kp[a]);
+  float s = v*v;
+  #pragma unroll
+  for (int off=32; off>0; off>>=1) s += __shfl_xor(s, off, 64);
+  if (d == 0) out[wv] = s;
 }
 
 __global__ __launch_bounds__(256) void m2norm(
@@ -933,23 +789,6 @@
   if (i == 0) nrm[bh] = red[0];
 }
 
-__global__ __launch_bounds__(256) void newton_init(
-    const float* __restrict__ M2, const float* __restrict__ nrm, float* __restrict__ inv)
-{
-  __shared__ float T[64][65];
-  int bh = blockIdx.x, i0 = blockIdx.y*64, j0 = blockIdx.z*64;
-  float nn = nrm[bh];
-  float sc = 1.0f/(nn*nn + 1e-6f);
-  const float* Mb = M2 + (size_t)bh*65536;
-  float* ob = inv + (size_t)bh*65536;
-  int t = threadIdx.x;
-  #pragma unroll
-  for (int e=0;e<16;e++){ int f=e*256+t; int r=f>>6, c=f&63; T[r][c] = Mb[(i0+r)*256 + j0+c]; }
-  __syncthreads();
-  #pragma unroll
-  for (int e=0;e<16;e++){ int f=e*256+t; int r=f>>6, c=f&63; ob[(j0+r)*256 + i0+c] = T[c][r]*sc; }
-}
-
 __global__ __launch_bounds__(256) void diag_fill(u16* out, int n, float val)
 {
   int i = blockIdx.x*256 + threadIdx.x;
@@ -968,159 +807,102 @@
   #define DUAL(kf, kb2) do { kf; kb2; } while(0)
 
   int* flag = (int*)d_ws;
+
+  char* base = (char*)d_ws;
+  size_t off = 256;
+  auto A = [&](size_t bytes)->char*{ char* r = base + off; off += (bytes + 255) & ~(size_t)255; return r; };
+  u16*  Xh = (u16*)A(XS_ELE*2);
+  u16*  Xl = (u16*)A(XS_ELE*2);
+  float* q  = (float*)A((size_t)BH*NSEQ*64*4);
+  char*  KT = A((size_t)6*32*65536*2*2);
+  float* XP = (float*)A((size_t)NBATCH*LM*768*4);
+  float* QL = (float*)A((size_t)BH*LM*64*4);
+  float* KL = (float*)A((size_t)BH*LM*64*4);
+  u16*  Wqh = (u16*)A((size_t)144*KB768*64*8*2);
+  u16*  Wql = (u16*)A((size_t)144*KB768*64*8*2);
+  u16*  Wph = (u16*)A((size_t)48*KB768*64*8*2);
+  u16*  Wpl = (u16*)A((size_t)48*KB768*64*8*2);
+  float* curF = (float*)A((size_t)32*65536*4);
+  float* bq  = (float*)A(2304*4);
+  float* bp  = (float*)A(768*4);
+  float* qn  = (float*)A((size_t)BH*NSEQ*4);
+  float* qln = (float*)A((size_t)BH*LM*4);
+  float* kln = (float*)A((size_t)BH*LM*4);
+  float* kpn = (float*)A((size_t)BH*NP*4);
+  float* nrm = (float*)A(256*4);
+  if (ws_size < off){
+    diag_fill<<<(out_size+255)/256, 256, 0, stream>>>((u16*)d_out, out_size, (float)(ws_size >> 20));
+    return;
+  }
+  float* M2 = (float*)Xh;
+  u16*  Yh = Xh;
+  u16*  Yl = Xh + XS_ELE;
+  float* KV = XP;
+  float* Vm = QL;
+  u16*  Kp = (u16*)KT;
+  u16*  Vp = (u16*)KT + (size_t)192*65536;
+  u16*  KLh = (u16*)XP;
+  u16*  KLl = KLh + (size_t)BH*16384;
+  u16*  Vmh = (u16*)KL;
+  u16*  Vml = Vmh + (size_t)BH*16384;
+  const size_t PB = (size_t)32*65536;
+  u16* nb = (u16*)KT;
+  u16 *curAh = nb + 0*2*PB, *curAl = curAh + PB;
+  u16 *curBh = nb + 1*2*PB, *curBl = curBh + PB;
+  u16 *TsBh  = nb + 2*2*PB, *TsBl  = TsBh  + PB;
+  u16 *nxtAh = nb + 3*2*PB, *nxtAl = nxtAh + PB;
+  u16 *nxtBh = nb + 4*2*PB, *nxtBl = nxtBh + PB;
+  u16 *M2Ah  = nb + 5*2*PB, *M2Al  = M2Ah  + PB;
+
   probe_dtype<<<1, 256, 0, stream>>>((const u16*)d_in[0], flag);
-
-  {
-    char* base = (char*)d_ws;
-    size_t off = 256;
-    auto A = [&](size_t bytes)->char*{ char* r = base + off; off += (bytes + 255) & ~(size_t)255; return r; };
-    u16*  Xh = (u16*)A(XS_ELE*2);
-    u16*  Xl = (u16*)A(XS_ELE*2);
-    float* q  = (float*)A((size_t)BH*NSEQ*64*4);
-    char*  KT = A((size_t)6*32*65536*2*2);
-    float* XP = (float*)A((size_t)NBATCH*LM*768*4);
-    float* QL = (float*)A((size_t)BH*LM*64*4);
-    float* KL = (float*)A((size_t)BH*LM*64*4);
-    u16*  Wqh = (u16*)A((size_t)144*KB768*64*8*2);
-    u16*  Wql = (u16*)A((size_t)144*KB768*64*8*2);
-    u16*  Wph = (u16*)A((size_t)48*KB768*64*8*2);
-    u16*  Wpl = (u16*)A((size_t)48*KB768*64*8*2);
-    float* curF = (float*)A((size_t)32*65536*4);
-    float* bq  = (float*)A(2304*4);
-    float* bp  = (float*)A(768*4);
-    float* qn  = (float*)A((size_t)BH*NSEQ*4);
-    float* qln = (float*)A((size_t)BH*LM*4);
-    float* kln = (float*)A((size_t)BH*LM*4);
-    float* kpn = (float*)A((size_t)BH*NP*4);
-    float* nrm = (float*)A(256*4);
-    if (ws_size >= off){
-      float* M2 = (float*)Xh;
-      u16*  Yh = Xh;
-      u16*  Yl = Xh + XS_ELE;
-      float* KV = XP;
-      float* Vm = QL;
-      u16* kp = (u16*)KT;
-      u16* vp = (u16*)(KT + (size_t)BH*NP*64*2);
-      const size_t PB = (size_t)32*65536;
-      u16* nb = (u16*)KT;
-      u16 *curAh = nb + 0*2*PB, *curAl = curAh + PB;
-      u16 *curBh = nb + 1*2*PB, *curBl = curBh + PB;
-      u16 *TsBh  = nb + 2*2*PB, *TsBl  = TsBh  + PB;
-      u16 *nxtAh = nb + 3*2*PB, *nxtAl = nxtAh + PB;
-      u16 *nxtBh = nb + 4*2*PB, *nxtBl = nxtBh + PB;
-      u16 *M2Ah  = nb + 5*2*PB, *M2Al  = M2Ah  + PB;
-
-      DUAL((cvt_bias<float><<<9,256,0,stream>>>(flag,0,bf,pbf,bq,bp)),
-           (cvt_bias<u16>  <<<9,256,0,stream>>>(flag,1,bb,pbb,bq,bp)));
-      DUAL((pack_ab<float><<<MT_X*KB768*64/256,256,0,stream>>>(flag,0,xf,MROWS,MT_X,Xh,Xl)),
-           (pack_ab<u16>  <<<MT_X*KB768*64/256,256,0,stream>>>(flag,1,xb,MROWS,MT_X,Xh,Xl)));
-      DUAL((pack_ab<float><<<144*KB768*64/256,256,0,stream>>>(flag,0,wf,2304,144,Wqh,Wql)),
-           (pack_ab<u16>  <<<144*KB768*64/256,256,0,stream>>>(flag,1,wb,2304,144,Wqh,Wql)));
-      DUAL((pack_ab<float><<<48*KB768*64/256,256,0,stream>>>(flag,0,pwf,768,48,Wph,Wpl)),
-           (pack_ab<u16>  <<<48*KB768*64/256,256,0,stream>>>(flag,1,pwb,768,48,Wph,Wpl)));
-      qkv_mfma<<<dim3(129,36),256,0,stream>>>(Xh,Xl,Wqh,Wql,bq,q,kp,vp);
-      DUAL((xpool<float><<<(NBATCH*LM*768)/256,256,0,stream>>>(flag,0,xf,XP)),
-           (xpool<u16>  <<<(NBATCH*LM*768)/256,256,0,stream>>>(flag,1,xb,XP)));
-      DUAL((lgemm<float><<<dim3(64,12),256,0,stream>>>(flag,0,XP,wf,bf,0,QL)),
-           (lgemm<u16>  <<<dim3(64,12),256,0,stream>>>(flag,1,XP,wb,bb,0,QL)));
-      DUAL((lgemm<float><<<dim3(64,12),256,0,stream>>>(flag,0,XP,wf,bf,768,KL)),
-           (lgemm<u16>  <<<dim3(64,12),256,0,stream>>>(flag,1,XP,wb,bb,768,KL)));
-      rownorm<float><<<(BH*LM*64)/256,256,0,stream>>>(QL, qln, BH*LM);
-      rownorm<float><<<(BH*LM*64)/256,256,0,stream>>>(KL, kln, BH*LM);
-      rownorm<float><<<(BH*NSEQ*64)/256,256,0,stream>>>(q, qn, BH*NSEQ);
-      rownorm<u16><<<(BH*NP*64)/256,256,0,stream>>>(kp, kpn, BH*NP);
-      gauss_m2<<<dim3(BH,4,4),256,0,stream>>>(QL, KL, qln, kln, M2);
-      m2norm<<<BH,256,0,stream>>>(M2, nrm);
-      gauss_av<0,256,1024,float,u16,u16><<<dim3(BH,4),256,0,stream>>>(QL, kp, vp, qln, kpn, KV);
-      for (int g = 0; g < 6; ++g){
-        const float* M2g = M2 + (size_t)g*32*65536;
-        pack_newtA<<<1024,256,0,stream>>>(M2g, M2Ah, M2Al);
-        newton_initP<<<dim3(32,4,4),256,0,stream>>>(M2g, nrm+g*32, curAh,curAl,curBh,curBl);
-        for (int it = 0; it < 6; ++it){
-          mgemmP<1><<<dim3(32,4,4),256,0,stream>>>(M2Ah,M2Al,curBh,curBl,
-                                                   nullptr,nullptr,TsBh,TsBl,nullptr);
-          if (it < 5){
-            mgemmP<0><<<dim3(32,4,4),256,0,stream>>>(curAh,curAl,TsBh,TsBl,
-                                                     nxtAh,nxtAl,nxtBh,nxtBl,nullptr);
-            u16* t0;
-            t0=curAh; curAh=nxtAh; nxtAh=t0;  t0=curAl; curAl=nxtAl; nxtAl=t0;
-            t0=curBh; curBh=nxtBh; nxtBh=t0;  t0=curBl; curBl=nxtBl; nxtBl=t0;
-          } else {
-            mgemmP<2><<<dim3(32,4,4),256,0,stream>>>(curAh,curAl,TsBh,TsBl,
-                                                     nullptr,nullptr,nullptr,nullptr,curF);
-          }
-        }
-        bgemm<0,64><<<dim3(32,4,1),256,0,stream>>>(curF, KV + (size_t)g*32*16384,
-                                                   Vm + (size_t)g*32*16384);
-      }
-      gauss_av<2,1025,256,float,float,float><<<dim3(BH,17),256,0,stream>>>(
-          q, KL, Vm, qn, kln, (float*)Yh);
-      DUAL((proj_mfma<float><<<dim3(129,12),256,0,stream>>>(flag,0,Yh,Yl,Wph,Wpl,bp,(float*)d_out)),
-           (proj_mfma<u16>  <<<dim3(129,12),256,0,stream>>>(flag,1,Yh,Yl,Wph,Wpl,bp,(u16*)d_out)));
-      return;
-    }
-  }
-
-  {
-    char* base = (char*)d_ws;
-    size_t off = 256;
-    auto A = [&](size_t bytes)->char*{ char* r = base + off; off += (bytes + 255) & ~(size_t)255; return r; };
-    float* XP   = (float*)A((size_t)NBATCH*LM*768*4);
-    float* QL   = (float*)A((size_t)BH*LM*64*4);
-    float* KL   = (float*)A((size_t)BH*LM*64*4);
-    char*  M2Y  = A((size_t)MROWS*768*4);
-    char*  KPV  = A((size_t)MROWS*768*4);
-    float* qn   = (float*)A((size_t)BH*NSEQ*4);
-    float* qln  = (float*)A((size_t)BH*LM*4);
-    float* kln  = (float*)A((size_t)BH*LM*4);
-    float* kpn  = (float*)A((size_t)BH*NP*4);
-    float* nrm  = (float*)A(256*4);
-    if (ws_size < off){
-      diag_fill<<<(out_size+255)/256, 256, 0, stream>>>((u16*)d_out, out_size, (float)(ws_size >> 20));
-      return;
-    }
-    float* M2 = (float*)M2Y;
-    float* y  = (float*)M2Y;
-    float* KV = XP;
-    float* Vm = QL;
-    u16*   kp = (u16*)KPV;
-    u16*   vp = (u16*)(KPV + (size_t)BH*NP*64*2);
-    float* T0 = (float*)KPV;
-    float* T1 = T0 + (size_t)64*65536;
-    float* T2 = T0 + (size_t)128*65536;
-    float* q  = (float*)KPV;
-
-    DUAL((xpool<float><<<(NBATCH*LM*768)/256,256,0,stream>>>(flag,0,xf,XP)),
-         (xpool<u16>  <<<(NBATCH*LM*768)/256,256,0,stream>>>(flag,1,xb,XP)));
-    DUAL((lgemm<float><<<dim3(64,12),256,0,stream>>>(flag,0,XP,wf,bf,0,QL)),
-         (lgemm<u16>  <<<dim3(64,12),256,0,stream>>>(flag,1,XP,wb,bb,0,QL)));
-    DUAL((lgemm<float><<<dim3(64,12),256,0,stream>>>(flag,0,XP,wf,bf,768,KL)),
-         (lgemm<u16>  <<<dim3(64,12),256,0,stream>>>(flag,1,XP,wb,bb,768,KL)));
-    rownorm<float><<<(BH*LM*64)/256,256,0,stream>>>(QL, qln, BH*LM);
-    rownorm<float><<<(BH*LM*64)/256,256,0,stream>>>(KL, kln, BH*LM);
-    gauss_m2<<<dim3(BH,4,4),256,0,stream>>>(QL, KL, qln, kln, M2);
-    m2norm<<<BH,256,0,stream>>>(M2, nrm);
-    DUAL((kvgemm<float><<<dim3(256,24),256,0,stream>>>(flag,0,xf,wf,bf,kp,vp)),
-         (kvgemm<u16>  <<<dim3(256,24),256,0,stream>>>(flag,1,xb,wb,bb,kp,vp)));
-    rownorm<u16><<<(BH*NP*64)/256,256,0,stream>>>(kp, kpn, BH*NP);
-    gauss_av<0,256,1024,float,u16,u16><<<dim3(BH,4),256,0,stream>>>(QL, kp, vp, qln, kpn, KV);
-    for (int g = 0; g < 3; ++g){
-      const float* M2g = M2 + (size_t)g*64*65536;
-      newton_init<<<dim3(64,4,4),256,0,stream>>>(M2g, nrm + g*64, T0);
-      float* cur = T0; float* nxt = T2;
-      for (int it = 0; it < 6; ++it){
-        mgemm<1><<<dim3(64,4,4),256,0,stream>>>(M2g, cur, T1);
-        mgemm<0><<<dim3(64,4,4),256,0,stream>>>(cur, T1, nxt);
-        float* tt = cur; cur = nxt; nxt = tt;
-      }
-      bgemm<0,64><<<dim3(64,4,1),256,0,stream>>>(cur, KV + (size_t)g*64*16384,
-                                                 Vm + (size_t)g*64*16384);
-    }
-    DUAL((qgemm<float><<<dim3(257,12),256,0,stream>>>(flag,0,xf,wf,bf,q)),
-         (qgemm<u16>  <<<dim3(257,12),256,0,stream>>>(flag,1,xb,wb,bb,q)));
-    rownorm<float><<<(BH*NSEQ*64)/256,256,0,stream>>>(q, qn, BH*NSEQ);
-    gauss_av<1,1025,256,float,float,float><<<dim3(BH,17),256,0,stream>>>(q, KL, Vm, qn, kln, y);
-    DUAL((projgemm<float><<<dim3(257,12),256,0,stream>>>(flag,0,y,pwf,pbf,(float*)d_out)),
-         (projgemm<u16>  <<<dim3(257,12),256,0,stream>>>(flag,1,y,pwb,pbb,(u16*)d_out)));
-  }
-}
+  DUAL((cvt_bias<float><<<9,256,0,stream>>>(flag,0,bf,pbf,bq,bp)),
+       (cvt_bias<u16>  <<<9,256,0,stream>>>(flag,1,bb,pbb,bq,bp)));
+  DUAL((pack_ab<float><<<MT_X*KB768*64/256,256,0,stream>>>(flag,0,xf,MROWS,MT_X,Xh,Xl)),
+       (pack_ab<u16>  <<<MT_X*KB768*64/256,256,0,stream>>>(flag,1,xb,MROWS,MT_X,Xh,Xl)));
+  DUAL((pack_ab<float><<<144*KB768*64/256,256,0,stream>>>(flag,0,wf,2304,144,Wqh,Wql)),
+       (pack_ab<u16>  <<<144*KB768*64/256,256,0,stream>>>(flag,1,wb,2304,144,Wqh,Wql)));
+  DUAL((pack_ab<float><<<48*KB768*64/256,256,0,stream>>>(flag,0,pwf,768,48,Wph,Wpl)),
+       (pack_ab<u16>  <<<48*KB768*64/256,256,0,stream>>>(flag,1,pwb,768,48,Wph,Wpl)));
+  qkv_mfma<<<dim3(36,129),256,0,stream>>>(Xh,Xl,Wqh,Wql,bq,q,Kp,Vp);
+  DUAL((xpool<float><<<(NBATCH*LM*768)/256,256,0,stream>>>(flag,0,xf,XP)),
+       (xpool<u16>  <<<(NBATCH*LM*768)/256,256,0,stream>>>(flag,1,xb,XP)));
+  DUAL((lgemm<float><<<dim3(64,12),256,0,stream>>>(flag,0,XP,wf,bf,0,QL)),
+       (lgemm<u16>  <<<dim3(64,12),256,0,stream>>>(flag,1,XP,wb,bb,0,QL)));
+  DUAL((lgemm<float><<<dim3(64,12),256,0,stream>>>(flag,0,XP,wf,bf,768,KL)),
+       (lgemm<u16>  <<<dim3(64,12),256,0,stream>>>(flag,1,XP,wb,bb,768,KL)));
+  rownorm<float><<<(BH*LM*64)/256,256,0,stream>>>(QL, qln, BH*LM);
+  rownorm<float><<<(BH*LM*64)/256,256,0,stream>>>(KL, kln, BH*LM);
+  rownorm<float><<<(BH*NSEQ*64)/256,256,0,stream>>>(q, qn, BH*NSEQ);
+  rownorm_kpack<<<(BH*NP*64)/256,256,0,stream>>>(Kp, kpn);
+  gauss_m2<<<dim3(BH,4,4),256,0,stream>>>(QL, KL, qln, kln, M2);
+  m2norm<<<BH,256,0,stream>>>(M2, nrm);
+  gauss_av_m<0,256,1024,0,0><<<dim3(BH,4),256,0,stream>>>(
+      QL, Kp, nullptr, Vp, nullptr, qln, kpn, KV);
+  for (int g = 0; g < 6; ++g){
+    const float* M2g = M2 + (size_t)g*32*65536;
+    pack_newtA<<<1024,256,0,stream>>>(M2g, M2Ah, M2Al);
+    newton_initP<<<dim3(32,4,4),256,0,stream>>>(M2g, nrm+g*32, curAh,curAl,curBh,curBl);
+    for (int it = 0; it < 6; ++it){
+      mgemmP<1><<<dim3(32,4,4),256,0,stream>>>(M2Ah,M2Al,curBh,curBl,
+                                               nullptr,nullptr,TsBh,TsBl,nullptr);
+      if (it < 5){
+        mgemmP<0><<<dim3(32,4,4),256,0,stream>>>(curAh,curAl,TsBh,TsBl,
+                                                 nxtAh,nxtAl,nxtBh,nxtBl,nullptr);
+        u16* t0;
+        t0=curAh; curAh=nxtAh; nxtAh=t0;  t0=curAl; curAl=nxtAl; nxtAl=t0;
+        t0=curBh; curBh=nxtBh; nxtBh=t0;  t0=curBl; curBl=nxtBl; nxtBl=t0;
+      } else {
+        mgemmP<2><<<dim3(32,4,4),256,0,stream>>>(curAh,curAl,TsBh,TsBl,
+                                                 nullptr,nullptr,nullptr,nullptr,curF);
+      }
+    }
+    bgemm<0,64><<<dim3(32,4,1),256,0,stream>>>(curF, KV + (size_t)g*32*16384,
+                                               Vm + (size_t)g*32*16384);
+  }
+  pack_bKL<<<BH*2048/256,256,0,stream>>>(KL, KLh, KLl);
+  pack_bVm<<<BH*2048/256,256,0,stream>>>(Vm, Vmh, Vml);
+  gauss_av_m<2,1025,256,1,1><<<dim3(BH,17),256,0,stream>>>(
+      q, KLh, KLl, Vmh, Vml, qn, kln, (float*)Yh);
+  DUAL((proj_mfma<float><<<dim3(12,129),256,0,stream>>>(flag,0,Yh,Yl,Wph,Wpl,bp,(float*)d_out)),
+       (proj_mfma<u16>  <<<dim3(12,129),256,0,stream>>>(flag,1,Yh,Yl,Wph,Wpl,bp,(u16*)d_out)));
+}
```

Result: faster. 1.984 ms (-15.4%).
